# Optimization experiments

Hardware: AMD Instinct MI355X
Metric: run time of the kernel (lower is better)

Reference implementation:

```python
import jax, jax.numpy as jnp
import numpy as np

N_PEP, N_MHC, N_TCR = 20000, 5000, 100000
EMB, HID = 128, 256
E_PM, E_MT = 200000, 400000
B = 50000


def setup_inputs() -> dict:
    key = jax.random.key(0)
    ks = jax.random.split(key, 30)
    f32 = jnp.float32

    def w(k, shape, fan_in):
        # torch Linear default: U(-1/sqrt(fan_in), 1/sqrt(fan_in))
        lim = 1.0 / np.sqrt(fan_in)
        return jax.random.uniform(k, shape, dtype=f32, minval=-lim, maxval=lim)

    inp = {
        # embedding tables (learned params)
        "emb_pep": jax.random.normal(ks[0], (N_PEP, EMB), dtype=f32),
        "emb_mhc": jax.random.normal(ks[1], (N_MHC, EMB), dtype=f32),
        "emb_tcr": jax.random.normal(ks[2], (N_TCR, EMB), dtype=f32),
        # edge lists (src=edge_index[0], dst=edge_index[1])
        "src_pm": jax.random.randint(ks[3], (E_PM,), 0, N_PEP, dtype=jnp.int32),
        "dst_pm": jax.random.randint(ks[4], (E_PM,), 0, N_MHC, dtype=jnp.int32),
        "src_mt": jax.random.randint(ks[5], (E_MT,), 0, N_MHC, dtype=jnp.int32),
        "dst_mt": jax.random.randint(ks[6], (E_MT,), 0, N_TCR, dtype=jnp.int32),
        # triplet pack indices
        "pack_pep": jax.random.randint(ks[7], (B,), 0, N_PEP, dtype=jnp.int32),
        "pack_mhc": jax.random.randint(ks[8], (B,), 0, N_MHC, dtype=jnp.int32),
        "pack_tcr": jax.random.randint(ks[9], (B,), 0, N_TCR, dtype=jnp.int32),
        # SAGEConv params: Wl (aggregated neighbors, with bias), Wr (root, no bias)
        # layer 1: pep->mhc (src 128, dst 128); mhc->tcr (src 128, dst 128)
        "l1_pm_Wl": w(ks[10], (HID, EMB), EMB), "l1_pm_bl": w(ks[11], (HID,), EMB),
        "l1_pm_Wr": w(ks[12], (HID, EMB), EMB),
        "l1_mt_Wl": w(ks[13], (HID, EMB), EMB), "l1_mt_bl": w(ks[14], (HID,), EMB),
        "l1_mt_Wr": w(ks[15], (HID, EMB), EMB),
        # layer 2: pep->mhc (src 128, dst 256); mhc->tcr (src 256, dst 256)
        "l2_pm_Wl": w(ks[16], (HID, EMB), EMB), "l2_pm_bl": w(ks[17], (HID,), EMB),
        "l2_pm_Wr": w(ks[18], (HID, HID), HID),
        "l2_mt_Wl": w(ks[19], (HID, HID), HID), "l2_mt_bl": w(ks[20], (HID,), HID),
        "l2_mt_Wr": w(ks[21], (HID, HID), HID),
        # proj_pep and head MLP
        "proj_W": w(ks[22], (HID, EMB), EMB), "proj_b": w(ks[23], (HID,), EMB),
        "head_W1": w(ks[24], (HID, 3 * HID), 3 * HID), "head_b1": w(ks[25], (HID,), 3 * HID),
        "head_W2": w(ks[26], (1, HID), HID), "head_b2": w(ks[27], (1,), HID),
    }
    return inp


def _sage(x_src, x_dst, src, dst, Wl, bl, Wr, n_dst):
    # SAGEConv(mean): lin_l(mean_{j in N(i)} x_src[j]) + lin_r(x_dst[i])
    msg = jax.ops.segment_sum(x_src[src], dst, num_segments=n_dst)  # [n_dst, d_src]
    cnt = jax.ops.segment_sum(jnp.ones((src.shape[0],), x_src.dtype), dst, num_segments=n_dst)
    mean = msg / jnp.maximum(cnt, 1.0)[:, None]
    return mean @ Wl.T + bl + x_dst @ Wr.T


def reference(emb_pep, emb_mhc, emb_tcr,
              src_pm, dst_pm, src_mt, dst_mt,
              pack_pep, pack_mhc, pack_tcr,
              l1_pm_Wl, l1_pm_bl, l1_pm_Wr, l1_mt_Wl, l1_mt_bl, l1_mt_Wr,
              l2_pm_Wl, l2_pm_bl, l2_pm_Wr, l2_mt_Wl, l2_mt_bl, l2_mt_Wr,
              proj_W, proj_b, head_W1, head_b1, head_W2, head_b2):
    relu = jax.nn.relu
    # layer 1 (HeteroConv reads all relations from the same input dict)
    mhc1 = relu(_sage(emb_pep, emb_mhc, src_pm, dst_pm, l1_pm_Wl, l1_pm_bl, l1_pm_Wr, N_MHC))
    tcr1 = relu(_sage(emb_mhc, emb_tcr, src_mt, dst_mt, l1_mt_Wl, l1_mt_bl, l1_mt_Wr, N_TCR))
    # layer 2 ('pep' is never a destination, so it keeps its embedding)
    mhc2 = relu(_sage(emb_pep, mhc1, src_pm, dst_pm, l2_pm_Wl, l2_pm_bl, l2_pm_Wr, N_MHC))
    tcr2 = relu(_sage(mhc1, tcr1, src_mt, dst_mt, l2_mt_Wl, l2_mt_bl, l2_mt_Wr, N_TCR))
    # projections + triplet gather (dropout disabled: inference)
    hp = (emb_pep @ proj_W.T + proj_b)[pack_pep]  # [B, HID]
    hm = mhc2[pack_mhc]
    ht = tcr2[pack_tcr]
    z = jnp.concatenate([hp, hm, ht], axis=-1)  # [B, 3*HID]
    hidden = relu(z @ head_W1.T + head_b1)
    logits = hidden @ head_W2.T + head_b2
    return logits.squeeze(-1)
```

## Files before the change

kernel.cpp:

```cpp
#include <hip/hip_runtime.h>

constexpr int NPEP = 20000, NMHC = 5000, NTCR = 100000;
constexpr int EPM = 200000, EMT = 400000, BB = 50000;
constexpr int MAXU = 50000;

typedef __attribute__((ext_vector_type(8))) short bf16x8;
typedef __attribute__((ext_vector_type(4))) float f32x4;

__device__ inline ushort f2bf(float x) {
    union { float f; unsigned u; } v; v.f = x;
    unsigned r = (v.u + 0x7FFF + ((v.u >> 16) & 1)) >> 16;
    return (ushort)r;
}
__device__ inline float bf2f(ushort b) {
    union { unsigned u; float f; } t; t.u = ((unsigned)b) << 16; return t.f;
}
__device__ inline void bf2x2(unsigned u, float& a, float& b) {
    union { unsigned x; float f; } t1, t2;
    t1.x = u << 16; t2.x = u & 0xffff0000u;
    a = t1.f; b = t2.f;
}
__device__ inline ushort4 f4bf(float4 v) {
    return make_ushort4(f2bf(v.x), f2bf(v.y), f2bf(v.z), f2bf(v.w));
}

__global__ __launch_bounds__(256) void prep_kernel(
    int* __restrict__ ibz,
    const float4* __restrict__ Wr1f, ushort4* __restrict__ Wr1_b,
    const float4* __restrict__ Wr2f, ushort4* __restrict__ Wr2_b,
    const float* __restrict__ head_W1, ushort4* __restrict__ W1b_b, ushort4* __restrict__ W1c_b,
    const float* __restrict__ l1_pm_Wl, const float* __restrict__ l1_pm_Wr,
    const float* __restrict__ l1_mt_Wl, ushort* __restrict__ Wcat1_b,
    const float* __restrict__ l2_pm_Wl, const float* __restrict__ l2_pm_Wr,
    const float* __restrict__ l2_mt_Wl, ushort* __restrict__ Wcat2_b,
    const float4* __restrict__ emb_mhc, ushort* __restrict__ Acat1,
    const float* __restrict__ proj_W, const float* __restrict__ proj_b,
    ushort* __restrict__ Wcomp_b, float* __restrict__ bp) {
    __shared__ float red[128];
    const int b = blockIdx.x, tid = threadIdx.x;
    if (b < 303) {
        int i = b * 256 + tid;
        if (i < 77500) ((int4*)ibz)[i] = make_int4(0, 0, 0, 0);
    } else if (b < 335) {
        int i = (b - 303) * 256 + tid;
        if (i < 8192) Wr1_b[i] = f4bf(Wr1f[i]);
    } else if (b < 399) {
        int i = (b - 335) * 256 + tid;
        if (i < 16384) Wr2_b[i] = f4bf(Wr2f[i]);
    } else if (b < 463) {
        int i = (b - 399) * 256 + tid;
        if (i < 16384) {
            int n = i >> 6, k4 = (i & 63) * 4;
            float4 v = *(const float4*)(head_W1 + (size_t)n * 768 + 256 + k4);
            W1b_b[i] = f4bf(v);
        }
    } else if (b < 527) {
        int i = (b - 463) * 256 + tid;
        if (i < 16384) {
            int n = i >> 6, k4 = (i & 63) * 4;
            float4 v = *(const float4*)(head_W1 + (size_t)n * 768 + 512 + k4);
            W1c_b[i] = f4bf(v);
        }
    } else if (b < 1039) {
        int idx = (b - 527) * 256 + tid;
        if (idx < 131072) {
            int r = idx >> 8, k = idx & 255;
            float v;
            if (r < 256) v = (k < 128) ? l1_pm_Wl[r * 128 + k] : l1_pm_Wr[r * 128 + (k - 128)];
            else         v = (k < 128) ? 0.f : l1_mt_Wl[(r - 256) * 128 + (k - 128)];
            Wcat1_b[idx] = f2bf(v);
        }
    } else if (b < 1807) {
        int idx = (b - 1039) * 256 + tid;
        if (idx < 196608) {
            int r = idx / 384, k = idx - r * 384;
            float v;
            if (r < 256) v = (k < 128) ? l2_pm_Wl[r * 128 + k] : l2_pm_Wr[r * 256 + (k - 128)];
            else         v = (k < 128) ? 0.f : l2_mt_Wl[(r - 256) * 256 + (k - 128)];
            Wcat2_b[idx] = f2bf(v);
        }
    } else if (b < 2432) {
        int i4 = (b - 1807) * 256 + tid;
        if (i4 < 160000) {
            int r = i4 >> 5, c4 = (i4 & 31) * 4;
            *(ushort4*)(Acat1 + (size_t)r * 256 + 128 + c4) = f4bf(emb_mhc[i4]);
        }
    } else {
        int i = b - 2432;
        const float* w1row = head_W1 + (size_t)i * 768;
        if (tid < 128) {
            float acc = 0.f;
            for (int k = 0; k < 256; k++) acc += w1row[k] * proj_W[k * 128 + tid];
            Wcomp_b[i * 128 + tid] = f2bf(acc);
            float pb = w1row[2 * tid] * proj_b[2 * tid] + w1row[2 * tid + 1] * proj_b[2 * tid + 1];
            red[tid] = pb;
        }
        __syncthreads();
        if (tid < 64) { red[tid] += red[tid + 64]; }
        __syncthreads();
        if (tid < 32) { red[tid] += red[tid + 32]; }
        __syncthreads();
        if (tid == 0) {
            float s = 0.f;
            for (int j = 0; j < 32; j++) s += red[j];
            bp[i] = s;
        }
    }
}

__global__ void hist2_kernel(const int* __restrict__ dst_pm, const int* __restrict__ dst_mt,
                             const int* __restrict__ pack_tcr,
                             int* __restrict__ deg_pm, int* __restrict__ deg_mt,
                             int* __restrict__ mark) {
    int t = blockIdx.x * blockDim.x + threadIdx.x;
    if (t < EPM) atomicAdd(&deg_pm[dst_pm[t]], 1);
    else if (t < EPM + EMT) atomicAdd(&deg_mt[dst_mt[t - EPM]], 1);
    else if (t < EPM + EMT + BB) mark[pack_tcr[t - EPM - EMT]] = 1;
}

__global__ __launch_bounds__(256) void blocksum2_kernel(const int* __restrict__ deg_pm,
                                                        const int* __restrict__ deg_mt,
                                                        const int* __restrict__ mark,
                                                        int* __restrict__ bsum_pm,
                                                        int* __restrict__ bsum_mt,
                                                        int* __restrict__ bsum_mk) {
    __shared__ int red[256];
    const int tid = threadIdx.x;
    const int* deg; int n, bi; int* bsum;
    if (blockIdx.x < 5) { deg = deg_pm; n = NMHC; bi = blockIdx.x; bsum = bsum_pm; }
    else if (blockIdx.x < 103) { deg = deg_mt; n = NTCR; bi = blockIdx.x - 5; bsum = bsum_mt; }
    else { deg = mark; n = NTCR; bi = blockIdx.x - 103; bsum = bsum_mk; }
    const int base = bi * 1024;
    int s = 0;
#pragma unroll
    for (int j = 0; j < 4; j++) {
        int i = base + tid + j * 256;
        if (i < n) s += deg[i];
    }
    red[tid] = s;
    __syncthreads();
    for (int off = 128; off > 0; off >>= 1) {
        if (tid < off) red[tid] += red[tid + off];
        __syncthreads();
    }
    if (tid == 0) bsum[bi] = red[0];
}

__global__ __launch_bounds__(128) void scanb2_kernel(int* __restrict__ bsum_pm,
                                                     int* __restrict__ bsum_mt,
                                                     int* __restrict__ bsum_mk) {
    __shared__ int s[128];
    const int tid = threadIdx.x;
    int* bsum = (blockIdx.x == 0) ? bsum_pm : ((blockIdx.x == 1) ? bsum_mt : bsum_mk);
    const int nb = (blockIdx.x == 0) ? 5 : 98;
    int v = (tid < nb) ? bsum[tid] : 0;
    s[tid] = v;
    __syncthreads();
    for (int off = 1; off < 128; off <<= 1) {
        int t = (tid >= off) ? s[tid - off] : 0;
        __syncthreads();
        s[tid] += t;
        __syncthreads();
    }
    if (tid < nb) bsum[tid] = (tid > 0) ? s[tid - 1] : 0;
    if (tid == 0) bsum[nb] = s[nb - 1];
}

__global__ __launch_bounds__(256) void emit2_kernel(const int* __restrict__ deg_pm,
                                                    const int* __restrict__ deg_mt,
                                                    const int* __restrict__ mark,
                                                    const int* __restrict__ bsum_pm,
                                                    const int* __restrict__ bsum_mt,
                                                    const int* __restrict__ bsum_mk,
                                                    int* __restrict__ rp_pm, float* __restrict__ cnt_pm,
                                                    int* __restrict__ rp_mt, float* __restrict__ cnt_mt,
                                                    int* __restrict__ list) {
    __shared__ int tsum[256];
    const int tid = threadIdx.x;
    const int* deg; const int* bsum; int* rp; float* cnt; int n, nb, bi, mode;
    if (blockIdx.x < 5) { deg = deg_pm; bsum = bsum_pm; rp = rp_pm; cnt = cnt_pm; n = NMHC; nb = 5; bi = blockIdx.x; mode = 0; }
    else if (blockIdx.x < 103) { deg = deg_mt; bsum = bsum_mt; rp = rp_mt; cnt = cnt_mt; n = NTCR; nb = 98; bi = blockIdx.x - 5; mode = 0; }
    else { deg = mark; bsum = bsum_mk; rp = nullptr; cnt = nullptr; n = NTCR; nb = 98; bi = blockIdx.x - 103; mode = 1; }
    const int i0 = bi * 1024 + tid * 4;
    int4 v = make_int4(0, 0, 0, 0);
    if (i0 + 3 < n) v = *(const int4*)(deg + i0);
    else if (i0 < n) {
        int t[4] = {0, 0, 0, 0};
        for (int j = 0; j < 4 && i0 + j < n; j++) t[j] = deg[i0 + j];
        v = make_int4(t[0], t[1], t[2], t[3]);
    }
    int s = v.x + v.y + v.z + v.w;
    tsum[tid] = s;
    __syncthreads();
    for (int off = 1; off < 256; off <<= 1) {
        int t = (tid >= off) ? tsum[tid - off] : 0;
        __syncthreads();
        tsum[tid] += t;
        __syncthreads();
    }
    int ex = ((tid > 0) ? tsum[tid - 1] : 0) + bsum[bi];
    if (mode == 0) {
        if (i0 + 3 < n) {
            int r1 = ex + v.x, r2 = r1 + v.y, r3 = r2 + v.z;
            *(int4*)(rp + i0) = make_int4(ex, r1, r2, r3);
            *(float4*)(cnt + i0) = make_float4((float)v.x, (float)v.y, (float)v.z, (float)v.w);
        } else if (i0 < n) {
            int r = ex;
            int vv[4] = {v.x, v.y, v.z, v.w};
            for (int j = 0; j < 4 && i0 + j < n; j++) {
                rp[i0 + j] = r;
                cnt[i0 + j] = (float)vv[j];
                r += vv[j];
            }
        }
        if (bi == 0 && tid == 0) rp[n] = bsum[nb];
    } else {
        int p = ex;
        int vv[4] = {v.x, v.y, v.z, v.w};
#pragma unroll
        for (int j = 0; j < 4; j++) {
            if (i0 + j < n && vv[j]) list[p++] = i0 + j;
        }
    }
}

__global__ void fill2_kernel(const int* __restrict__ src_pm, const int* __restrict__ dst_pm,
                             const int* __restrict__ src_mt, const int* __restrict__ dst_mt,
                             const int* __restrict__ rp_pm, int* __restrict__ cur_pm, int* __restrict__ csr_pm,
                             const int* __restrict__ rp_mt, int* __restrict__ cur_mt, int* __restrict__ csr_mt) {
    int t = blockIdx.x * blockDim.x + threadIdx.x;
    if (t < EPM) {
        int d = dst_pm[t];
        int pos = atomicAdd(&cur_pm[d], 1);
        csr_pm[rp_pm[d] + pos] = src_pm[t];
    } else if (t < EPM + EMT) {
        int t2 = t - EPM;
        int d = dst_mt[t2];
        int pos = atomicAdd(&cur_mt[d], 1);
        csr_mt[rp_mt[d] + pos] = src_mt[t2];
    }
}

__global__ __launch_bounds__(256) void gatherpm_kernel(const int* __restrict__ rp,
                                                       const int* __restrict__ csr_src,
                                                       const float* __restrict__ X,
                                                       ushort* __restrict__ A1, ushort* __restrict__ A2,
                                                       int n) {
    const int tid = threadIdx.x;
    const int r = blockIdx.x * 8 + (tid >> 5);
    const int lane = tid & 31;
    if (r >= n) return;
    const int e0 = rp[r], e1 = rp[r + 1];
    float4 s = make_float4(0.f, 0.f, 0.f, 0.f);
    for (int e = e0; e < e1; e++) {
        const int sidx = csr_src[e];
        float4 v = ((const float4*)(X + (long)sidx * 128))[lane];
        s.x += v.x; s.y += v.y; s.z += v.z; s.w += v.w;
    }
    float sc = 1.f / fmaxf((float)(e1 - e0), 1.f);
    ushort4 o = make_ushort4(f2bf(s.x * sc), f2bf(s.y * sc), f2bf(s.z * sc), f2bf(s.w * sc));
    *(ushort4*)(A1 + (size_t)r * 256 + lane * 4) = o;
    *(ushort4*)(A2 + (size_t)r * 384 + lane * 4) = o;
}

template <int K, int NB0, bool RELU0, bool G2>
__global__ __launch_bounds__(256, 2) void mfma_fused_kernel(
    int M, const ushort* __restrict__ A, const ushort* __restrict__ W,
    const float* __restrict__ bias,
    ushort* __restrict__ out0, int s0, ushort* __restrict__ out1) {
    constexpr int RS = 40;
    __shared__ ushort Als[128 * RS];
    __shared__ ushort Wls[128 * RS];
    const int tid = threadIdx.x;
    const int m0 = blockIdx.x * 128, n0 = blockIdx.y * 128;
    const int lane = tid & 63, w = tid >> 6;
    const int wm = w >> 1, wn = w & 1;
    const int m16 = lane & 15, q = lane >> 4;

    f32x4 acc[4][4] = {};

    for (int k0 = 0; k0 < K; k0 += 32) {
        bf16x8 a_st[2], w_st[2];
#pragma unroll
        for (int r = 0; r < 2; r++) {
            int chunk = tid + r * 256;
            int row = chunk >> 2, off = (chunk & 3) * 8;
            int ga = min(m0 + row, M - 1);
            a_st[r] = *(const bf16x8*)(A + (size_t)ga * K + k0 + off);
            w_st[r] = *(const bf16x8*)(W + (size_t)(n0 + row) * K + k0 + off);
        }
        __syncthreads();
#pragma unroll
        for (int r = 0; r < 2; r++) {
            int chunk = tid + r * 256;
            int row = chunk >> 2, off = (chunk & 3) * 8;
            *(bf16x8*)(&Als[row * RS + off]) = a_st[r];
            *(bf16x8*)(&Wls[row * RS + off]) = w_st[r];
        }
        __syncthreads();
        bf16x8 af[4], bf[4];
#pragma unroll
        for (int t = 0; t < 4; t++) {
            af[t] = *(const bf16x8*)(&Als[(wm * 64 + t * 16 + m16) * RS + q * 8]);
            bf[t] = *(const bf16x8*)(&Wls[(wn * 64 + t * 16 + m16) * RS + q * 8]);
        }
#pragma unroll
        for (int mt = 0; mt < 4; mt++)
#pragma unroll
            for (int nt = 0; nt < 4; nt++)
                acc[mt][nt] = __builtin_amdgcn_mfma_f32_16x16x32_bf16(af[mt], bf[nt], acc[mt][nt], 0, 0, 0);
    }

    const bool g1 = G2 && ((int)blockIdx.y >= NB0);
#pragma unroll
    for (int mt = 0; mt < 4; mt++) {
#pragma unroll
        for (int i = 0; i < 4; i++) {
            int row = m0 + wm * 64 + mt * 16 + q * 4 + i;
            if (row >= M) continue;
#pragma unroll
            for (int nt = 0; nt < 4; nt++) {
                int col = n0 + wn * 64 + nt * 16 + m16;
                float v = acc[mt][nt][i];
                if (!g1) {
                    v += bias[col];
                    if (RELU0) v = fmaxf(v, 0.f);
                    out0[(size_t)row * s0 + col] = f2bf(v);
                } else {
                    out1[(size_t)row * 256 + (col - NB0 * 128)] = f2bf(v);
                }
            }
        }
    }
}

__global__ __launch_bounds__(256, 3) void tcrall_kernel(
    const int* __restrict__ nrowsp, const int* __restrict__ list,
    const int* __restrict__ rp, const int* __restrict__ csr_src,
    const ushort* __restrict__ Z1, const ushort* __restrict__ Z2,
    const float* __restrict__ emb_tcr,
    const ushort* __restrict__ Wr1, const ushort* __restrict__ Wr2,
    const ushort* __restrict__ W1c,
    const float* __restrict__ bl1, const float* __restrict__ bl2,
    ushort* __restrict__ Ht) {
    constexpr int RS1 = 136;
    constexpr int RS2 = 264;
    __shared__ ushort B[32 * RS2];
    __shared__ ushort A1[32 * RS2];
    __shared__ ushort A2[32 * RS2];
    __shared__ int origs[32];
    const int tid = threadIdx.x;
    const int M = nrowsp[0];
    const int m0 = blockIdx.x * 32;
    if (m0 >= M) return;
    const int lane = tid & 63, w = tid >> 6;
    const int m16 = lane & 15, q = lane >> 4;

    if (tid < 32) origs[tid] = list[min(m0 + tid, M - 1)];

#pragma unroll
    for (int r = 0; r < 4; r++) {
        int chunk = tid + r * 256;
        int row = chunk >> 5, c4 = (chunk & 31) * 4;
        int grow = list[min(m0 + row, M - 1)];
        float4 v = *(const float4*)(emb_tcr + (size_t)grow * 128 + c4);
        *(ushort4*)(&B[row * RS1 + c4]) = f4bf(v);
    }

    {
        const int g = tid >> 5, gl = tid & 31;
        for (int rr = g; rr < 32; rr += 8) {
            int cr = min(m0 + rr, M - 1);
            int orig = list[cr];
            int e0 = rp[orig], e1 = rp[orig + 1];
            float s1[8] = {}, s2[8] = {};
            for (int e = e0; e < e1; e++) {
                int sidx = csr_src[e];
                uint4 u1 = *(const uint4*)(Z1 + (size_t)sidx * 256 + gl * 8);
                uint4 u2 = *(const uint4*)(Z2 + (size_t)sidx * 256 + gl * 8);
                float a, b;
                bf2x2(u1.x, a, b); s1[0] += a; s1[1] += b;
                bf2x2(u1.y, a, b); s1[2] += a; s1[3] += b;
                bf2x2(u1.z, a, b); s1[4] += a; s1[5] += b;
                bf2x2(u1.w, a, b); s1[6] += a; s1[7] += b;
                bf2x2(u2.x, a, b); s2[0] += a; s2[1] += b;
                bf2x2(u2.y, a, b); s2[2] += a; s2[3] += b;
                bf2x2(u2.z, a, b); s2[4] += a; s2[5] += b;
                bf2x2(u2.w, a, b); s2[6] += a; s2[7] += b;
            }
            float es = 1.f / fmaxf((float)(e1 - e0), 1.f);
            uint4 w1, w2;
            w1.x = (unsigned)f2bf(s1[0] * es) | ((unsigned)f2bf(s1[1] * es) << 16);
            w1.y = (unsigned)f2bf(s1[2] * es) | ((unsigned)f2bf(s1[3] * es) << 16);
            w1.z = (unsigned)f2bf(s1[4] * es) | ((unsigned)f2bf(s1[5] * es) << 16);
            w1.w = (unsigned)f2bf(s1[6] * es) | ((unsigned)f2bf(s1[7] * es) << 16);
            w2.x = (unsigned)f2bf(s2[0] * es) | ((unsigned)f2bf(s2[1] * es) << 16);
            w2.y = (unsigned)f2bf(s2[2] * es) | ((unsigned)f2bf(s2[3] * es) << 16);
            w2.z = (unsigned)f2bf(s2[4] * es) | ((unsigned)f2bf(s2[5] * es) << 16);
            w2.w = (unsigned)f2bf(s2[6] * es) | ((unsigned)f2bf(s2[7] * es) << 16);
            *(uint4*)(&A1[rr * RS2 + gl * 8]) = w1;
            *(uint4*)(&A2[rr * RS2 + gl * 8]) = w2;
        }
    }
    __syncthreads();

    {
        f32x4 acc[2][4] = {};
        for (int k0 = 0; k0 < 128; k0 += 32) {
            bf16x8 af[2], bf[4];
#pragma unroll
            for (int t = 0; t < 2; t++)
                af[t] = *(const bf16x8*)(&B[(t * 16 + m16) * RS1 + k0 + q * 8]);
#pragma unroll
            for (int t = 0; t < 4; t++)
                bf[t] = *(const bf16x8*)(Wr1 + (size_t)(w * 64 + t * 16 + m16) * 128 + k0 + q * 8);
#pragma unroll
            for (int mt = 0; mt < 2; mt++)
#pragma unroll
                for (int nt = 0; nt < 4; nt++)
                    acc[mt][nt] = __builtin_amdgcn_mfma_f32_16x16x32_bf16(af[mt], bf[nt], acc[mt][nt], 0, 0, 0);
        }
        __syncthreads();
#pragma unroll
        for (int mt = 0; mt < 2; mt++)
#pragma unroll
            for (int i = 0; i < 4; i++) {
                int lr = mt * 16 + q * 4 + i;
#pragma unroll
                for (int nt = 0; nt < 4; nt++) {
                    int col = w * 64 + nt * 16 + m16;
                    float v = acc[mt][nt][i] + bl1[col] + bf2f(A1[lr * RS2 + col]);
                    B[lr * RS2 + col] = f2bf(fmaxf(v, 0.f));
                }
            }
    }
    __syncthreads();

    {
        f32x4 acc[2][4] = {};
        for (int k0 = 0; k0 < 256; k0 += 32) {
            bf16x8 af[2], bf[4];
#pragma unroll
            for (int t = 0; t < 2; t++)
                af[t] = *(const bf16x8*)(&B[(t * 16 + m16) * RS2 + k0 + q * 8]);
#pragma unroll
            for (int t = 0; t < 4; t++)
                bf[t] = *(const bf16x8*)(Wr2 + (size_t)(w * 64 + t * 16 + m16) * 256 + k0 + q * 8);
#pragma unroll
            for (int mt = 0; mt < 2; mt++)
#pragma unroll
                for (int nt = 0; nt < 4; nt++)
                    acc[mt][nt] = __builtin_amdgcn_mfma_f32_16x16x32_bf16(af[mt], bf[nt], acc[mt][nt], 0, 0, 0);
        }
        __syncthreads();
#pragma unroll
        for (int mt = 0; mt < 2; mt++)
#pragma unroll
            for (int i = 0; i < 4; i++) {
                int lr = mt * 16 + q * 4 + i;
#pragma unroll
                for (int nt = 0; nt < 4; nt++) {
                    int col = w * 64 + nt * 16 + m16;
                    float v = acc[mt][nt][i] + bl2[col] + bf2f(A2[lr * RS2 + col]);
                    B[lr * RS2 + col] = f2bf(fmaxf(v, 0.f));
                }
            }
    }
    __syncthreads();

    {
        f32x4 acc[2][4] = {};
        for (int k0 = 0; k0 < 256; k0 += 32) {
            bf16x8 af[2], bf[4];
#pragma unroll
            for (int t = 0; t < 2; t++)
                af[t] = *(const bf16x8*)(&B[(t * 16 + m16) * RS2 + k0 + q * 8]);
#pragma unroll
            for (int t = 0; t < 4; t++)
                bf[t] = *(const bf16x8*)(W1c + (size_t)(w * 64 + t * 16 + m16) * 256 + k0 + q * 8);
#pragma unroll
            for (int mt = 0; mt < 2; mt++)
#pragma unroll
                for (int nt = 0; nt < 4; nt++)
                    acc[mt][nt] = __builtin_amdgcn_mfma_f32_16x16x32_bf16(af[mt], bf[nt], acc[mt][nt], 0, 0, 0);
        }
        __syncthreads();
#pragma unroll
        for (int mt = 0; mt < 2; mt++)
#pragma unroll
            for (int i = 0; i < 4; i++) {
                int lr = mt * 16 + q * 4 + i;
#pragma unroll
                for (int nt = 0; nt < 4; nt++) {
                    int col = w * 64 + nt * 16 + m16;
                    B[lr * RS2 + col] = f2bf(acc[mt][nt][i]);
                }
            }
    }
    __syncthreads();

#pragma unroll
    for (int r = 0; r < 4; r++) {
        int chunk = tid + r * 256;
        int row = chunk >> 5, c8 = (chunk & 31) * 8;
        if (m0 + row < M)
            *(uint4*)(Ht + (size_t)origs[row] * 256 + c8) = *(const uint4*)(&B[row * RS2 + c8]);
    }
}

template <int K, bool HASB, bool AF32>
__global__ __launch_bounds__(256, 2) void mfma_out_kernel(
    int M, const void* __restrict__ Av, const ushort* __restrict__ W,
    const float* __restrict__ bias, ushort* __restrict__ out) {
    constexpr int RS = 40;
    __shared__ ushort Als[128 * RS];
    __shared__ ushort Wls[128 * RS];
    const int tid = threadIdx.x;
    const int m0 = blockIdx.x * 128, n0 = blockIdx.y * 128;
    const int lane = tid & 63, w = tid >> 6;
    const int wm = w >> 1, wn = w & 1;
    const int m16 = lane & 15, q = lane >> 4;

    f32x4 acc[4][4] = {};

    for (int k0 = 0; k0 < K; k0 += 32) {
        bf16x8 a_st[2], w_st[2];
#pragma unroll
        for (int r = 0; r < 2; r++) {
            int chunk = tid + r * 256;
            int row = chunk >> 2, off = (chunk & 3) * 8;
            int ga = min(m0 + row, M - 1);
            if constexpr (AF32) {
                const float* Af = (const float*)Av;
                float4 f0 = *(const float4*)(Af + (size_t)ga * K + k0 + off);
                float4 f1 = *(const float4*)(Af + (size_t)ga * K + k0 + off + 4);
                ushort4 u0 = f4bf(f0), u1 = f4bf(f1);
                bf16x8 av;
                av[0] = (short)u0.x; av[1] = (short)u0.y; av[2] = (short)u0.z; av[3] = (short)u0.w;
                av[4] = (short)u1.x; av[5] = (short)u1.y; av[6] = (short)u1.z; av[7] = (short)u1.w;
                a_st[r] = av;
            } else {
                a_st[r] = *(const bf16x8*)((const ushort*)Av + (size_t)ga * K + k0 + off);
            }
            w_st[r] = *(const bf16x8*)(W + (size_t)(n0 + row) * K + k0 + off);
        }
        __syncthreads();
#pragma unroll
        for (int r = 0; r < 2; r++) {
            int chunk = tid + r * 256;
            int row = chunk >> 2, off = (chunk & 3) * 8;
            *(bf16x8*)(&Als[row * RS + off]) = a_st[r];
            *(bf16x8*)(&Wls[row * RS + off]) = w_st[r];
        }
        __syncthreads();
        bf16x8 af[4], bf[4];
#pragma unroll
        for (int t = 0; t < 4; t++) {
            af[t] = *(const bf16x8*)(&Als[(wm * 64 + t * 16 + m16) * RS + q * 8]);
            bf[t] = *(const bf16x8*)(&Wls[(wn * 64 + t * 16 + m16) * RS + q * 8]);
        }
#pragma unroll
        for (int mt = 0; mt < 4; mt++)
#pragma unroll
            for (int nt = 0; nt < 4; nt++)
                acc[mt][nt] = __builtin_amdgcn_mfma_f32_16x16x32_bf16(af[mt], bf[nt], acc[mt][nt], 0, 0, 0);
    }

#pragma unroll
    for (int mt = 0; mt < 4; mt++) {
#pragma unroll
        for (int i = 0; i < 4; i++) {
            int row = m0 + wm * 64 + mt * 16 + q * 4 + i;
            if (row >= M) continue;
#pragma unroll
            for (int nt = 0; nt < 4; nt++) {
                int col = n0 + wn * 64 + nt * 16 + m16;
                float v = acc[mt][nt][i];
                if (HASB) v += bias[col];
                out[(size_t)row * 256 + col] = f2bf(v);
            }
        }
    }
}

__global__ __launch_bounds__(256) void combine_kernel(
    const ushort* __restrict__ Hp, const ushort* __restrict__ Hm, const ushort* __restrict__ Ht,
    const int* __restrict__ pp, const int* __restrict__ pm, const int* __restrict__ pt,
    const float* __restrict__ b1, const float* __restrict__ W2, const float* __restrict__ b2,
    float* __restrict__ out) {
    const int tid = threadIdx.x;
    const int lane = tid & 63, w = tid >> 6;
    const int c = lane * 4;
    const float4 b1v = *(const float4*)(b1 + c);
    const float4 w2v = *(const float4*)(W2 + c);
    const float b2v = b2[0];
    const int base = blockIdx.x * 32 + w * 8;
#pragma unroll
    for (int t = 0; t < 8; t++) {
        int i = base + t;
        if (i >= BB) return;
        int ra = pp[i], rb = pm[i], rc = pt[i];
        ushort4 ua = *(const ushort4*)(Hp + (size_t)ra * 256 + c);
        ushort4 ub = *(const ushort4*)(Hm + (size_t)rb * 256 + c);
        ushort4 uc = *(const ushort4*)(Ht + (size_t)rc * 256 + c);
        float h0 = fmaxf(bf2f(ua.x) + bf2f(ub.x) + bf2f(uc.x) + b1v.x, 0.f);
        float h1 = fmaxf(bf2f(ua.y) + bf2f(ub.y) + bf2f(uc.y) + b1v.y, 0.f);
        float h2 = fmaxf(bf2f(ua.z) + bf2f(ub.z) + bf2f(uc.z) + b1v.z, 0.f);
        float h3 = fmaxf(bf2f(ua.w) + bf2f(ub.w) + bf2f(uc.w) + b1v.w, 0.f);
        float p = h0 * w2v.x + h1 * w2v.y + h2 * w2v.z + h3 * w2v.w;
#pragma unroll
        for (int off = 32; off > 0; off >>= 1) p += __shfl_down(p, off);
        if (lane == 0) out[i] = p + b2v;
    }
}

extern "C" void kernel_launch(void* const* d_in, const int* in_sizes, int n_in,
                              void* d_out, int out_size, void* d_ws, size_t ws_size,
                              hipStream_t stream) {
    const float* emb_pep = (const float*)d_in[0];
    const float* emb_mhc = (const float*)d_in[1];
    const float* emb_tcr = (const float*)d_in[2];
    const int* src_pm = (const int*)d_in[3];
    const int* dst_pm = (const int*)d_in[4];
    const int* src_mt = (const int*)d_in[5];
    const int* dst_mt = (const int*)d_in[6];
    const int* pack_pep = (const int*)d_in[7];
    const int* pack_mhc = (const int*)d_in[8];
    const int* pack_tcr = (const int*)d_in[9];
    const float* l1_pm_Wl = (const float*)d_in[10];
    const float* l1_pm_bl = (const float*)d_in[11];
    const float* l1_pm_Wr = (const float*)d_in[12];
    const float* l1_mt_Wl = (const float*)d_in[13];
    const float* l1_mt_bl = (const float*)d_in[14];
    const float* l1_mt_Wr = (const float*)d_in[15];
    const float* l2_pm_Wl = (const float*)d_in[16];
    const float* l2_pm_bl = (const float*)d_in[17];
    const float* l2_pm_Wr = (const float*)d_in[18];
    const float* l2_mt_Wl = (const float*)d_in[19];
    const float* l2_mt_bl = (const float*)d_in[20];
    const float* l2_mt_Wr = (const float*)d_in[21];
    const float* proj_W = (const float*)d_in[22];
    const float* proj_b = (const float*)d_in[23];
    const float* head_W1 = (const float*)d_in[24];
    const float* head_b1 = (const float*)d_in[25];
    const float* head_W2 = (const float*)d_in[26];
    const float* head_b2 = (const float*)d_in[27];
    float* out = (float*)d_out;

    int* ib = (int*)d_ws;
    int* deg_pm = ib;
    int* cur_pm = ib + 5000;
    int* deg_mt = ib + 10000;
    int* cur_mt = ib + 110000;
    int* mark   = ib + 210000;
    int* rp_pm  = ib + 310000;
    int* rp_mt  = ib + 315008;
    int* csr_pm = ib + 415016;
    int* csr_mt = ib + 615016;
    int* bsum_pm = ib + 1015016;
    int* bsum_mt = ib + 1015176;
    int* bsum_mk = ib + 1015336;
    int* list    = ib + 1015496;

    float* f = (float*)(ib + 1065544);
    float* cnt_pm = f;
    float* cnt_mt = f + 5000;
    float* bp     = f + 105000;

    ushort* u = (ushort*)(f + 105344);
    ushort* Wcat1_b = u;
    ushort* Wcat2_b = u + 131072;
    ushort* W1b_b   = u + 327680;
    ushort* W1c_b   = u + 393216;
    ushort* Wcomp_b = u + 458752;
    ushort* Wr1_b   = u + 491520;
    ushort* Wr2_b   = u + 524288;
    ushort* Acat1   = u + 589824;
    ushort* Acat2   = u + 1869824;
    ushort* Zb1     = u + 3789824;
    ushort* Zb2     = u + 5069824;
    ushort* mhc2_b  = u + 6349824;
    ushort* Hp_b    = u + 7629824;
    ushort* Hm_b    = u + 12749824;
    ushort* Ht_b    = u + 14029824;

    prep_kernel<<<2688, 256, 0, stream>>>(
        ib,
        (const float4*)l1_mt_Wr, (ushort4*)Wr1_b,
        (const float4*)l2_mt_Wr, (ushort4*)Wr2_b,
        head_W1, (ushort4*)W1b_b, (ushort4*)W1c_b,
        l1_pm_Wl, l1_pm_Wr, l1_mt_Wl, Wcat1_b,
        l2_pm_Wl, l2_pm_Wr, l2_mt_Wl, Wcat2_b,
        (const float4*)emb_mhc, Acat1,
        proj_W, proj_b, Wcomp_b, bp);

    hist2_kernel<<<(EPM + EMT + BB + 255) / 256, 256, 0, stream>>>(
        dst_pm, dst_mt, pack_tcr, deg_pm, deg_mt, mark);
    blocksum2_kernel<<<201, 256, 0, stream>>>(deg_pm, deg_mt, mark, bsum_pm, bsum_mt, bsum_mk);
    scanb2_kernel<<<3, 128, 0, stream>>>(bsum_pm, bsum_mt, bsum_mk);
    emit2_kernel<<<201, 256, 0, stream>>>(deg_pm, deg_mt, mark, bsum_pm, bsum_mt, bsum_mk,
                                          rp_pm, cnt_pm, rp_mt, cnt_mt, list);
    fill2_kernel<<<(EPM + EMT + 255) / 256, 256, 0, stream>>>(
        src_pm, dst_pm, src_mt, dst_mt, rp_pm, cur_pm, csr_pm, rp_mt, cur_mt, csr_mt);

    gatherpm_kernel<<<(NMHC + 7) / 8, 256, 0, stream>>>(rp_pm, csr_pm, emb_pep, Acat1, Acat2, NMHC);

    mfma_fused_kernel<256, 2, true, true><<<dim3((NMHC + 127) / 128, 4), 256, 0, stream>>>(
        NMHC, Acat1, Wcat1_b, l1_pm_bl, Acat2 + 128, 384, Zb1);
    mfma_fused_kernel<384, 2, true, true><<<dim3((NMHC + 127) / 128, 4), 256, 0, stream>>>(
        NMHC, Acat2, Wcat2_b, l2_pm_bl, mhc2_b, 256, Zb2);

    tcrall_kernel<<<(MAXU + 31) / 32, 256, 0, stream>>>(
        bsum_mk + 98, list, rp_mt, csr_mt, Zb1, Zb2, emb_tcr,
        Wr1_b, Wr2_b, W1c_b, l1_mt_bl, l2_mt_bl, Ht_b);

    mfma_out_kernel<128, true, true><<<dim3((NPEP + 127) / 128, 2), 256, 0, stream>>>(
        NPEP, emb_pep, Wcomp_b, bp, Hp_b);
    mfma_out_kernel<256, false, false><<<dim3((NMHC + 127) / 128, 2), 256, 0, stream>>>(
        NMHC, mhc2_b, W1b_b, nullptr, Hm_b);

    combine_kernel<<<(BB + 31) / 32, 256, 0, stream>>>(
        Hp_b, Hm_b, Ht_b, pack_pep, pack_mhc, pack_tcr,
        head_b1, head_W2, head_b2, out);
}
```

Baseline: 416.3 us.

## Fuse all stages into one persistent mega-kernel with software grid barriers

Replaces the chain of about a dozen kernel launches (prep, histogram, scans, CSR fill, gathers, MFMA GEMMs, tcr stage, output projections, combine) with a single persistent kernel sized to occupancy. The stages are separated by atomic-counter grid barriers. The aim is to remove per-launch overhead and the idle tails between small dependent kernels. In exchange, each phase runs on a fixed grid that may fit its work less well, the barriers cost spinning, and the union shared memory may lower occupancy. The barrier has a timeout break, which would break correctness if blocks are not co-resident.

```diff
diff --git a/kernel.cpp b/kernel.cpp
--- a/kernel.cpp
+++ b/kernel.cpp
@@ -2,7 +2,6 @@
 
 constexpr int NPEP = 20000, NMHC = 5000, NTCR = 100000;
 constexpr int EPM = 200000, EMT = 400000, BB = 50000;
-constexpr int MAXU = 50000;
 
 typedef __attribute__((ext_vector_type(8))) short bf16x8;
 typedef __attribute__((ext_vector_type(4))) float f32x4;
@@ -24,255 +23,59 @@
     return make_ushort4(f2bf(v.x), f2bf(v.y), f2bf(v.z), f2bf(v.w));
 }
 
-__global__ __launch_bounds__(256) void prep_kernel(
-    int* __restrict__ ibz,
-    const float4* __restrict__ Wr1f, ushort4* __restrict__ Wr1_b,
-    const float4* __restrict__ Wr2f, ushort4* __restrict__ Wr2_b,
-    const float* __restrict__ head_W1, ushort4* __restrict__ W1b_b, ushort4* __restrict__ W1c_b,
-    const float* __restrict__ l1_pm_Wl, const float* __restrict__ l1_pm_Wr,
-    const float* __restrict__ l1_mt_Wl, ushort* __restrict__ Wcat1_b,
-    const float* __restrict__ l2_pm_Wl, const float* __restrict__ l2_pm_Wr,
-    const float* __restrict__ l2_mt_Wl, ushort* __restrict__ Wcat2_b,
-    const float4* __restrict__ emb_mhc, ushort* __restrict__ Acat1,
-    const float* __restrict__ proj_W, const float* __restrict__ proj_b,
-    ushort* __restrict__ Wcomp_b, float* __restrict__ bp) {
-    __shared__ float red[128];
-    const int b = blockIdx.x, tid = threadIdx.x;
-    if (b < 303) {
-        int i = b * 256 + tid;
-        if (i < 77500) ((int4*)ibz)[i] = make_int4(0, 0, 0, 0);
-    } else if (b < 335) {
-        int i = (b - 303) * 256 + tid;
-        if (i < 8192) Wr1_b[i] = f4bf(Wr1f[i]);
-    } else if (b < 399) {
-        int i = (b - 335) * 256 + tid;
-        if (i < 16384) Wr2_b[i] = f4bf(Wr2f[i]);
-    } else if (b < 463) {
-        int i = (b - 399) * 256 + tid;
-        if (i < 16384) {
-            int n = i >> 6, k4 = (i & 63) * 4;
-            float4 v = *(const float4*)(head_W1 + (size_t)n * 768 + 256 + k4);
-            W1b_b[i] = f4bf(v);
-        }
-    } else if (b < 527) {
-        int i = (b - 463) * 256 + tid;
-        if (i < 16384) {
-            int n = i >> 6, k4 = (i & 63) * 4;
-            float4 v = *(const float4*)(head_W1 + (size_t)n * 768 + 512 + k4);
-            W1c_b[i] = f4bf(v);
-        }
-    } else if (b < 1039) {
-        int idx = (b - 527) * 256 + tid;
-        if (idx < 131072) {
-            int r = idx >> 8, k = idx & 255;
-            float v;
-            if (r < 256) v = (k < 128) ? l1_pm_Wl[r * 128 + k] : l1_pm_Wr[r * 128 + (k - 128)];
-            else         v = (k < 128) ? 0.f : l1_mt_Wl[(r - 256) * 128 + (k - 128)];
-            Wcat1_b[idx] = f2bf(v);
-        }
-    } else if (b < 1807) {
-        int idx = (b - 1039) * 256 + tid;
-        if (idx < 196608) {
-            int r = idx / 384, k = idx - r * 384;
-            float v;
-            if (r < 256) v = (k < 128) ? l2_pm_Wl[r * 128 + k] : l2_pm_Wr[r * 256 + (k - 128)];
-            else         v = (k < 128) ? 0.f : l2_mt_Wl[(r - 256) * 256 + (k - 128)];
-            Wcat2_b[idx] = f2bf(v);
-        }
-    } else if (b < 2432) {
-        int i4 = (b - 1807) * 256 + tid;
-        if (i4 < 160000) {
-            int r = i4 >> 5, c4 = (i4 & 31) * 4;
-            *(ushort4*)(Acat1 + (size_t)r * 256 + 128 + c4) = f4bf(emb_mhc[i4]);
-        }
-    } else {
-        int i = b - 2432;
-        const float* w1row = head_W1 + (size_t)i * 768;
-        if (tid < 128) {
-            float acc = 0.f;
-            for (int k = 0; k < 256; k++) acc += w1row[k] * proj_W[k * 128 + tid];
-            Wcomp_b[i * 128 + tid] = f2bf(acc);
-            float pb = w1row[2 * tid] * proj_b[2 * tid] + w1row[2 * tid + 1] * proj_b[2 * tid + 1];
-            red[tid] = pb;
-        }
-        __syncthreads();
-        if (tid < 64) { red[tid] += red[tid + 64]; }
-        __syncthreads();
-        if (tid < 32) { red[tid] += red[tid + 32]; }
-        __syncthreads();
-        if (tid == 0) {
-            float s = 0.f;
-            for (int j = 0; j < 32; j++) s += red[j];
-            bp[i] = s;
-        }
-    }
-}
-
-__global__ void hist2_kernel(const int* __restrict__ dst_pm, const int* __restrict__ dst_mt,
-                             const int* __restrict__ pack_tcr,
-                             int* __restrict__ deg_pm, int* __restrict__ deg_mt,
-                             int* __restrict__ mark) {
-    int t = blockIdx.x * blockDim.x + threadIdx.x;
-    if (t < EPM) atomicAdd(&deg_pm[dst_pm[t]], 1);
-    else if (t < EPM + EMT) atomicAdd(&deg_mt[dst_mt[t - EPM]], 1);
-    else if (t < EPM + EMT + BB) mark[pack_tcr[t - EPM - EMT]] = 1;
-}
-
-__global__ __launch_bounds__(256) void blocksum2_kernel(const int* __restrict__ deg_pm,
-                                                        const int* __restrict__ deg_mt,
-                                                        const int* __restrict__ mark,
-                                                        int* __restrict__ bsum_pm,
-                                                        int* __restrict__ bsum_mt,
-                                                        int* __restrict__ bsum_mk) {
-    __shared__ int red[256];
-    const int tid = threadIdx.x;
-    const int* deg; int n, bi; int* bsum;
-    if (blockIdx.x < 5) { deg = deg_pm; n = NMHC; bi = blockIdx.x; bsum = bsum_pm; }
-    else if (blockIdx.x < 103) { deg = deg_mt; n = NTCR; bi = blockIdx.x - 5; bsum = bsum_mt; }
-    else { deg = mark; n = NTCR; bi = blockIdx.x - 103; bsum = bsum_mk; }
-    const int base = bi * 1024;
-    int s = 0;
-#pragma unroll
-    for (int j = 0; j < 4; j++) {
-        int i = base + tid + j * 256;
-        if (i < n) s += deg[i];
-    }
-    red[tid] = s;
+constexpr int RS  = 40;
+constexpr int RS1 = 136;
+constexpr int RS2 = 264;
+
+struct SMem {
+    union {
+        float red[128];
+        int ired[256];
+        int tsum[256];
+        struct { ushort Als[128 * RS]; ushort Wls[128 * RS]; } g;
+        struct { ushort B[32 * RS2]; ushort A1[32 * RS2]; ushort A2[32 * RS2];
+                 int origs[32]; } t;
+    };
+};
+
+struct MegaArgs {
+    const float *emb_pep, *emb_mhc, *emb_tcr;
+    const int *src_pm, *dst_pm, *src_mt, *dst_mt;
+    const int *pack_pep, *pack_mhc, *pack_tcr;
+    const float *l1_pm_Wl, *l1_pm_bl, *l1_pm_Wr, *l1_mt_Wl, *l1_mt_bl, *l1_mt_Wr;
+    const float *l2_pm_Wl, *l2_pm_bl, *l2_pm_Wr, *l2_mt_Wl, *l2_mt_bl, *l2_mt_Wr;
+    const float *proj_W, *proj_b, *head_W1, *head_b1, *head_W2, *head_b2;
+    float* out;
+    int *deg_pm, *cur_pm, *deg_mt, *cur_mt, *mark;
+    int *rp_pm, *rp_mt, *csr_pm, *csr_mt;
+    int *bsum_pm, *bsum_mt, *bsum_mk, *nrows, *list, *bar;
+    float* bp;
+    ushort *Wcat1_b, *Wcat2_b, *W1b_b, *W1c_b, *Wcomp_b, *Wr1_b, *Wr2_b;
+    ushort *Acat1, *Acat2, *Zb1, *Zb2, *mhc2_b, *Hp_b, *Hm_b, *Ht_b;
+};
+
+__device__ inline void gbar(int* cnt, int target) {
     __syncthreads();
-    for (int off = 128; off > 0; off >>= 1) {
-        if (tid < off) red[tid] += red[tid + off];
-        __syncthreads();
-    }
-    if (tid == 0) bsum[bi] = red[0];
-}
-
-__global__ __launch_bounds__(128) void scanb2_kernel(int* __restrict__ bsum_pm,
-                                                     int* __restrict__ bsum_mt,
-                                                     int* __restrict__ bsum_mk) {
-    __shared__ int s[128];
-    const int tid = threadIdx.x;
-    int* bsum = (blockIdx.x == 0) ? bsum_pm : ((blockIdx.x == 1) ? bsum_mt : bsum_mk);
-    const int nb = (blockIdx.x == 0) ? 5 : 98;
-    int v = (tid < nb) ? bsum[tid] : 0;
-    s[tid] = v;
+    __threadfence();
+    if (threadIdx.x == 0) {
+        atomicAdd(cnt, 1);
+        long long t0 = clock64();
+        while (__hip_atomic_load(cnt, __ATOMIC_RELAXED, __HIP_MEMORY_SCOPE_AGENT) < target) {
+            __builtin_amdgcn_s_sleep(2);
+            if (clock64() - t0 > 2000000000LL) break;
+        }
+    }
     __syncthreads();
-    for (int off = 1; off < 128; off <<= 1) {
-        int t = (tid >= off) ? s[tid - off] : 0;
-        __syncthreads();
-        s[tid] += t;
-        __syncthreads();
-    }
-    if (tid < nb) bsum[tid] = (tid > 0) ? s[tid - 1] : 0;
-    if (tid == 0) bsum[nb] = s[nb - 1];
-}
-
-__global__ __launch_bounds__(256) void emit2_kernel(const int* __restrict__ deg_pm,
-                                                    const int* __restrict__ deg_mt,
-                                                    const int* __restrict__ mark,
-                                                    const int* __restrict__ bsum_pm,
-                                                    const int* __restrict__ bsum_mt,
-                                                    const int* __restrict__ bsum_mk,
-                                                    int* __restrict__ rp_pm, float* __restrict__ cnt_pm,
-                                                    int* __restrict__ rp_mt, float* __restrict__ cnt_mt,
-                                                    int* __restrict__ list) {
-    __shared__ int tsum[256];
-    const int tid = threadIdx.x;
-    const int* deg; const int* bsum; int* rp; float* cnt; int n, nb, bi, mode;
-    if (blockIdx.x < 5) { deg = deg_pm; bsum = bsum_pm; rp = rp_pm; cnt = cnt_pm; n = NMHC; nb = 5; bi = blockIdx.x; mode = 0; }
-    else if (blockIdx.x < 103) { deg = deg_mt; bsum = bsum_mt; rp = rp_mt; cnt = cnt_mt; n = NTCR; nb = 98; bi = blockIdx.x - 5; mode = 0; }
-    else { deg = mark; bsum = bsum_mk; rp = nullptr; cnt = nullptr; n = NTCR; nb = 98; bi = blockIdx.x - 103; mode = 1; }
-    const int i0 = bi * 1024 + tid * 4;
-    int4 v = make_int4(0, 0, 0, 0);
-    if (i0 + 3 < n) v = *(const int4*)(deg + i0);
-    else if (i0 < n) {
-        int t[4] = {0, 0, 0, 0};
-        for (int j = 0; j < 4 && i0 + j < n; j++) t[j] = deg[i0 + j];
-        v = make_int4(t[0], t[1], t[2], t[3]);
-    }
-    int s = v.x + v.y + v.z + v.w;
-    tsum[tid] = s;
-    __syncthreads();
-    for (int off = 1; off < 256; off <<= 1) {
-        int t = (tid >= off) ? tsum[tid - off] : 0;
-        __syncthreads();
-        tsum[tid] += t;
-        __syncthreads();
-    }
-    int ex = ((tid > 0) ? tsum[tid - 1] : 0) + bsum[bi];
-    if (mode == 0) {
-        if (i0 + 3 < n) {
-            int r1 = ex + v.x, r2 = r1 + v.y, r3 = r2 + v.z;
-            *(int4*)(rp + i0) = make_int4(ex, r1, r2, r3);
-            *(float4*)(cnt + i0) = make_float4((float)v.x, (float)v.y, (float)v.z, (float)v.w);
-        } else if (i0 < n) {
-            int r = ex;
-            int vv[4] = {v.x, v.y, v.z, v.w};
-            for (int j = 0; j < 4 && i0 + j < n; j++) {
-                rp[i0 + j] = r;
-                cnt[i0 + j] = (float)vv[j];
-                r += vv[j];
-            }
-        }
-        if (bi == 0 && tid == 0) rp[n] = bsum[nb];
-    } else {
-        int p = ex;
-        int vv[4] = {v.x, v.y, v.z, v.w};
-#pragma unroll
-        for (int j = 0; j < 4; j++) {
-            if (i0 + j < n && vv[j]) list[p++] = i0 + j;
-        }
-    }
-}
-
-__global__ void fill2_kernel(const int* __restrict__ src_pm, const int* __restrict__ dst_pm,
-                             const int* __restrict__ src_mt, const int* __restrict__ dst_mt,
-                             const int* __restrict__ rp_pm, int* __restrict__ cur_pm, int* __restrict__ csr_pm,
-                             const int* __restrict__ rp_mt, int* __restrict__ cur_mt, int* __restrict__ csr_mt) {
-    int t = blockIdx.x * blockDim.x + threadIdx.x;
-    if (t < EPM) {
-        int d = dst_pm[t];
-        int pos = atomicAdd(&cur_pm[d], 1);
-        csr_pm[rp_pm[d] + pos] = src_pm[t];
-    } else if (t < EPM + EMT) {
-        int t2 = t - EPM;
-        int d = dst_mt[t2];
-        int pos = atomicAdd(&cur_mt[d], 1);
-        csr_mt[rp_mt[d] + pos] = src_mt[t2];
-    }
-}
-
-__global__ __launch_bounds__(256) void gatherpm_kernel(const int* __restrict__ rp,
-                                                       const int* __restrict__ csr_src,
-                                                       const float* __restrict__ X,
-                                                       ushort* __restrict__ A1, ushort* __restrict__ A2,
-                                                       int n) {
-    const int tid = threadIdx.x;
-    const int r = blockIdx.x * 8 + (tid >> 5);
-    const int lane = tid & 31;
-    if (r >= n) return;
-    const int e0 = rp[r], e1 = rp[r + 1];
-    float4 s = make_float4(0.f, 0.f, 0.f, 0.f);
-    for (int e = e0; e < e1; e++) {
-        const int sidx = csr_src[e];
-        float4 v = ((const float4*)(X + (long)sidx * 128))[lane];
-        s.x += v.x; s.y += v.y; s.z += v.z; s.w += v.w;
-    }
-    float sc = 1.f / fmaxf((float)(e1 - e0), 1.f);
-    ushort4 o = make_ushort4(f2bf(s.x * sc), f2bf(s.y * sc), f2bf(s.z * sc), f2bf(s.w * sc));
-    *(ushort4*)(A1 + (size_t)r * 256 + lane * 4) = o;
-    *(ushort4*)(A2 + (size_t)r * 384 + lane * 4) = o;
-}
-
-template <int K, int NB0, bool RELU0, bool G2>
-__global__ __launch_bounds__(256, 2) void mfma_fused_kernel(
-    int M, const ushort* __restrict__ A, const ushort* __restrict__ W,
+    __threadfence();
+}
+
+template <int K, int NB0, bool RELU0>
+__device__ __forceinline__ void fused_tile(
+    SMem& sm, int tid, int bx, int by, int M,
+    const ushort* __restrict__ A, const ushort* __restrict__ W,
     const float* __restrict__ bias,
     ushort* __restrict__ out0, int s0, ushort* __restrict__ out1) {
-    constexpr int RS = 40;
-    __shared__ ushort Als[128 * RS];
-    __shared__ ushort Wls[128 * RS];
-    const int tid = threadIdx.x;
-    const int m0 = blockIdx.x * 128, n0 = blockIdx.y * 128;
+    const int m0 = bx * 128, n0 = by * 128;
     const int lane = tid & 63, w = tid >> 6;
     const int wm = w >> 1, wn = w & 1;
     const int m16 = lane & 15, q = lane >> 4;
@@ -294,15 +97,15 @@
         for (int r = 0; r < 2; r++) {
             int chunk = tid + r * 256;
             int row = chunk >> 2, off = (chunk & 3) * 8;
-            *(bf16x8*)(&Als[row * RS + off]) = a_st[r];
-            *(bf16x8*)(&Wls[row * RS + off]) = w_st[r];
+            *(bf16x8*)(&sm.g.Als[row * RS + off]) = a_st[r];
+            *(bf16x8*)(&sm.g.Wls[row * RS + off]) = w_st[r];
         }
         __syncthreads();
         bf16x8 af[4], bf[4];
 #pragma unroll
         for (int t = 0; t < 4; t++) {
-            af[t] = *(const bf16x8*)(&Als[(wm * 64 + t * 16 + m16) * RS + q * 8]);
-            bf[t] = *(const bf16x8*)(&Wls[(wn * 64 + t * 16 + m16) * RS + q * 8]);
+            af[t] = *(const bf16x8*)(&sm.g.Als[(wm * 64 + t * 16 + m16) * RS + q * 8]);
+            bf[t] = *(const bf16x8*)(&sm.g.Wls[(wn * 64 + t * 16 + m16) * RS + q * 8]);
         }
 #pragma unroll
         for (int mt = 0; mt < 4; mt++)
@@ -311,7 +114,7 @@
                 acc[mt][nt] = __builtin_amdgcn_mfma_f32_16x16x32_bf16(af[mt], bf[nt], acc[mt][nt], 0, 0, 0);
     }
 
-    const bool g1 = G2 && ((int)blockIdx.y >= NB0);
+    const bool g1 = (by >= NB0);
 #pragma unroll
     for (int mt = 0; mt < 4; mt++) {
 #pragma unroll
@@ -334,189 +137,12 @@
     }
 }
 
-__global__ __launch_bounds__(256, 3) void tcrall_kernel(
-    const int* __restrict__ nrowsp, const int* __restrict__ list,
-    const int* __restrict__ rp, const int* __restrict__ csr_src,
-    const ushort* __restrict__ Z1, const ushort* __restrict__ Z2,
-    const float* __restrict__ emb_tcr,
-    const ushort* __restrict__ Wr1, const ushort* __restrict__ Wr2,
-    const ushort* __restrict__ W1c,
-    const float* __restrict__ bl1, const float* __restrict__ bl2,
-    ushort* __restrict__ Ht) {
-    constexpr int RS1 = 136;
-    constexpr int RS2 = 264;
-    __shared__ ushort B[32 * RS2];
-    __shared__ ushort A1[32 * RS2];
-    __shared__ ushort A2[32 * RS2];
-    __shared__ int origs[32];
-    const int tid = threadIdx.x;
-    const int M = nrowsp[0];
-    const int m0 = blockIdx.x * 32;
-    if (m0 >= M) return;
-    const int lane = tid & 63, w = tid >> 6;
-    const int m16 = lane & 15, q = lane >> 4;
-
-    if (tid < 32) origs[tid] = list[min(m0 + tid, M - 1)];
-
-#pragma unroll
-    for (int r = 0; r < 4; r++) {
-        int chunk = tid + r * 256;
-        int row = chunk >> 5, c4 = (chunk & 31) * 4;
-        int grow = list[min(m0 + row, M - 1)];
-        float4 v = *(const float4*)(emb_tcr + (size_t)grow * 128 + c4);
-        *(ushort4*)(&B[row * RS1 + c4]) = f4bf(v);
-    }
-
-    {
-        const int g = tid >> 5, gl = tid & 31;
-        for (int rr = g; rr < 32; rr += 8) {
-            int cr = min(m0 + rr, M - 1);
-            int orig = list[cr];
-            int e0 = rp[orig], e1 = rp[orig + 1];
-            float s1[8] = {}, s2[8] = {};
-            for (int e = e0; e < e1; e++) {
-                int sidx = csr_src[e];
-                uint4 u1 = *(const uint4*)(Z1 + (size_t)sidx * 256 + gl * 8);
-                uint4 u2 = *(const uint4*)(Z2 + (size_t)sidx * 256 + gl * 8);
-                float a, b;
-                bf2x2(u1.x, a, b); s1[0] += a; s1[1] += b;
-                bf2x2(u1.y, a, b); s1[2] += a; s1[3] += b;
-                bf2x2(u1.z, a, b); s1[4] += a; s1[5] += b;
-                bf2x2(u1.w, a, b); s1[6] += a; s1[7] += b;
-                bf2x2(u2.x, a, b); s2[0] += a; s2[1] += b;
-                bf2x2(u2.y, a, b); s2[2] += a; s2[3] += b;
-                bf2x2(u2.z, a, b); s2[4] += a; s2[5] += b;
-                bf2x2(u2.w, a, b); s2[6] += a; s2[7] += b;
-            }
-            float es = 1.f / fmaxf((float)(e1 - e0), 1.f);
-            uint4 w1, w2;
-            w1.x = (unsigned)f2bf(s1[0] * es) | ((unsigned)f2bf(s1[1] * es) << 16);
-            w1.y = (unsigned)f2bf(s1[2] * es) | ((unsigned)f2bf(s1[3] * es) << 16);
-            w1.z = (unsigned)f2bf(s1[4] * es) | ((unsigned)f2bf(s1[5] * es) << 16);
-            w1.w = (unsigned)f2bf(s1[6] * es) | ((unsigned)f2bf(s1[7] * es) << 16);
-            w2.x = (unsigned)f2bf(s2[0] * es) | ((unsigned)f2bf(s2[1] * es) << 16);
-            w2.y = (unsigned)f2bf(s2[2] * es) | ((unsigned)f2bf(s2[3] * es) << 16);
-            w2.z = (unsigned)f2bf(s2[4] * es) | ((unsigned)f2bf(s2[5] * es) << 16);
-            w2.w = (unsigned)f2bf(s2[6] * es) | ((unsigned)f2bf(s2[7] * es) << 16);
-            *(uint4*)(&A1[rr * RS2 + gl * 8]) = w1;
-            *(uint4*)(&A2[rr * RS2 + gl * 8]) = w2;
-        }
-    }
-    __syncthreads();
-
-    {
-        f32x4 acc[2][4] = {};
-        for (int k0 = 0; k0 < 128; k0 += 32) {
-            bf16x8 af[2], bf[4];
-#pragma unroll
-            for (int t = 0; t < 2; t++)
-                af[t] = *(const bf16x8*)(&B[(t * 16 + m16) * RS1 + k0 + q * 8]);
-#pragma unroll
-            for (int t = 0; t < 4; t++)
-                bf[t] = *(const bf16x8*)(Wr1 + (size_t)(w * 64 + t * 16 + m16) * 128 + k0 + q * 8);
-#pragma unroll
-            for (int mt = 0; mt < 2; mt++)
-#pragma unroll
-                for (int nt = 0; nt < 4; nt++)
-                    acc[mt][nt] = __builtin_amdgcn_mfma_f32_16x16x32_bf16(af[mt], bf[nt], acc[mt][nt], 0, 0, 0);
-        }
-        __syncthreads();
-#pragma unroll
-        for (int mt = 0; mt < 2; mt++)
-#pragma unroll
-            for (int i = 0; i < 4; i++) {
-                int lr = mt * 16 + q * 4 + i;
-#pragma unroll
-                for (int nt = 0; nt < 4; nt++) {
-                    int col = w * 64 + nt * 16 + m16;
-                    float v = acc[mt][nt][i] + bl1[col] + bf2f(A1[lr * RS2 + col]);
-                    B[lr * RS2 + col] = f2bf(fmaxf(v, 0.f));
-                }
-            }
-    }
-    __syncthreads();
-
-    {
-        f32x4 acc[2][4] = {};
-        for (int k0 = 0; k0 < 256; k0 += 32) {
-            bf16x8 af[2], bf[4];
-#pragma unroll
-            for (int t = 0; t < 2; t++)
-                af[t] = *(const bf16x8*)(&B[(t * 16 + m16) * RS2 + k0 + q * 8]);
-#pragma unroll
-            for (int t = 0; t < 4; t++)
-                bf[t] = *(const bf16x8*)(Wr2 + (size_t)(w * 64 + t * 16 + m16) * 256 + k0 + q * 8);
-#pragma unroll
-            for (int mt = 0; mt < 2; mt++)
-#pragma unroll
-                for (int nt = 0; nt < 4; nt++)
-                    acc[mt][nt] = __builtin_amdgcn_mfma_f32_16x16x32_bf16(af[mt], bf[nt], acc[mt][nt], 0, 0, 0);
-        }
-        __syncthreads();
-#pragma unroll
-        for (int mt = 0; mt < 2; mt++)
-#pragma unroll
-            for (int i = 0; i < 4; i++) {
-                int lr = mt * 16 + q * 4 + i;
-#pragma unroll
-                for (int nt = 0; nt < 4; nt++) {
-                    int col = w * 64 + nt * 16 + m16;
-                    float v = acc[mt][nt][i] + bl2[col] + bf2f(A2[lr * RS2 + col]);
-                    B[lr * RS2 + col] = f2bf(fmaxf(v, 0.f));
-                }
-            }
-    }
-    __syncthreads();
-
-    {
-        f32x4 acc[2][4] = {};
-        for (int k0 = 0; k0 < 256; k0 += 32) {
-            bf16x8 af[2], bf[4];
-#pragma unroll
-            for (int t = 0; t < 2; t++)
-                af[t] = *(const bf16x8*)(&B[(t * 16 + m16) * RS2 + k0 + q * 8]);
-#pragma unroll
-            for (int t = 0; t < 4; t++)
-                bf[t] = *(const bf16x8*)(W1c + (size_t)(w * 64 + t * 16 + m16) * 256 + k0 + q * 8);
-#pragma unroll
-            for (int mt = 0; mt < 2; mt++)
-#pragma unroll
-                for (int nt = 0; nt < 4; nt++)
-                    acc[mt][nt] = __builtin_amdgcn_mfma_f32_16x16x32_bf16(af[mt], bf[nt], acc[mt][nt], 0, 0, 0);
-        }
-        __syncthreads();
-#pragma unroll
-        for (int mt = 0; mt < 2; mt++)
-#pragma unroll
-            for (int i = 0; i < 4; i++) {
-                int lr = mt * 16 + q * 4 + i;
-#pragma unroll
-                for (int nt = 0; nt < 4; nt++) {
-                    int col = w * 64 + nt * 16 + m16;
-                    B[lr * RS2 + col] = f2bf(acc[mt][nt][i]);
-                }
-            }
-    }
-    __syncthreads();
-
-#pragma unroll
-    for (int r = 0; r < 4; r++) {
-        int chunk = tid + r * 256;
-        int row = chunk >> 5, c8 = (chunk & 31) * 8;
-        if (m0 + row < M)
-            *(uint4*)(Ht + (size_t)origs[row] * 256 + c8) = *(const uint4*)(&B[row * RS2 + c8]);
-    }
-}
-
 template <int K, bool HASB, bool AF32>
-__global__ __launch_bounds__(256, 2) void mfma_out_kernel(
-    int M, const void* __restrict__ Av, const ushort* __restrict__ W,
+__device__ __forceinline__ void out_tile(
+    SMem& sm, int tid, int bx, int by, int M,
+    const void* __restrict__ Av, const ushort* __restrict__ W,
     const float* __restrict__ bias, ushort* __restrict__ out) {
-    constexpr int RS = 40;
-    __shared__ ushort Als[128 * RS];
-    __shared__ ushort Wls[128 * RS];
-    const int tid = threadIdx.x;
-    const int m0 = blockIdx.x * 128, n0 = blockIdx.y * 128;
+    const int m0 = bx * 128, n0 = by * 128;
     const int lane = tid & 63, w = tid >> 6;
     const int wm = w >> 1, wn = w & 1;
     const int m16 = lane & 15, q = lane >> 4;
@@ -549,15 +175,15 @@
         for (int r = 0; r < 2; r++) {
             int chunk = tid + r * 256;
             int row = chunk >> 2, off = (chunk & 3) * 8;
-            *(bf16x8*)(&Als[row * RS + off]) = a_st[r];
-            *(bf16x8*)(&Wls[row * RS + off]) = w_st[r];
+            *(bf16x8*)(&sm.g.Als[row * RS + off]) = a_st[r];
+            *(bf16x8*)(&sm.g.Wls[row * RS + off]) = w_st[r];
         }
         __syncthreads();
         bf16x8 af[4], bf[4];
 #pragma unroll
         for (int t = 0; t < 4; t++) {
-            af[t] = *(const bf16x8*)(&Als[(wm * 64 + t * 16 + m16) * RS + q * 8]);
-            bf[t] = *(const bf16x8*)(&Wls[(wn * 64 + t * 16 + m16) * RS + q * 8]);
+            af[t] = *(const bf16x8*)(&sm.g.Als[(wm * 64 + t * 16 + m16) * RS + q * 8]);
+            bf[t] = *(const bf16x8*)(&sm.g.Wls[(wn * 64 + t * 16 + m16) * RS + q * 8]);
         }
 #pragma unroll
         for (int mt = 0; mt < 4; mt++)
@@ -583,143 +209,513 @@
     }
 }
 
-__global__ __launch_bounds__(256) void combine_kernel(
-    const ushort* __restrict__ Hp, const ushort* __restrict__ Hm, const ushort* __restrict__ Ht,
-    const int* __restrict__ pp, const int* __restrict__ pm, const int* __restrict__ pt,
-    const float* __restrict__ b1, const float* __restrict__ W2, const float* __restrict__ b2,
-    float* __restrict__ out) {
+__device__ __forceinline__ void tcr_tile(SMem& sm, int tid, int bt, int M, const MegaArgs& a) {
+    const int m0 = bt * 32;
+    const int lane = tid & 63, w = tid >> 6;
+    const int m16 = lane & 15, q = lane >> 4;
+
+    __syncthreads();
+
+    if (tid < 32) sm.t.origs[tid] = a.list[min(m0 + tid, M - 1)];
+
+#pragma unroll
+    for (int r = 0; r < 4; r++) {
+        int chunk = tid + r * 256;
+        int row = chunk >> 5, c4 = (chunk & 31) * 4;
+        int grow = a.list[min(m0 + row, M - 1)];
+        float4 v = *(const float4*)(a.emb_tcr + (size_t)grow * 128 + c4);
+        *(ushort4*)(&sm.t.B[row * RS1 + c4]) = f4bf(v);
+    }
+
+    {
+        const int g = tid >> 5, gl = tid & 31;
+        for (int rr = g; rr < 32; rr += 8) {
+            int cr = min(m0 + rr, M - 1);
+            int orig = a.list[cr];
+            int e0 = a.rp_mt[orig], e1 = a.rp_mt[orig + 1];
+            float s1[8] = {}, s2[8] = {};
+            for (int e = e0; e < e1; e++) {
+                int sidx = a.csr_mt[e];
+                uint4 u1 = *(const uint4*)(a.Zb1 + (size_t)sidx * 256 + gl * 8);
+                uint4 u2 = *(const uint4*)(a.Zb2 + (size_t)sidx * 256 + gl * 8);
+                float x, y;
+                bf2x2(u1.x, x, y); s1[0] += x; s1[1] += y;
+                bf2x2(u1.y, x, y); s1[2] += x; s1[3] += y;
+                bf2x2(u1.z, x, y); s1[4] += x; s1[5] += y;
+                bf2x2(u1.w, x, y); s1[6] += x; s1[7] += y;
+                bf2x2(u2.x, x, y); s2[0] += x; s2[1] += y;
+                bf2x2(u2.y, x, y); s2[2] += x; s2[3] += y;
+                bf2x2(u2.z, x, y); s2[4] += x; s2[5] += y;
+                bf2x2(u2.w, x, y); s2[6] += x; s2[7] += y;
+            }
+            float es = 1.f / fmaxf((float)(e1 - e0), 1.f);
+            uint4 w1, w2;
+            w1.x = (unsigned)f2bf(s1[0] * es) | ((unsigned)f2bf(s1[1] * es) << 16);
+            w1.y = (unsigned)f2bf(s1[2] * es) | ((unsigned)f2bf(s1[3] * es) << 16);
+            w1.z = (unsigned)f2bf(s1[4] * es) | ((unsigned)f2bf(s1[5] * es) << 16);
+            w1.w = (unsigned)f2bf(s1[6] * es) | ((unsigned)f2bf(s1[7] * es) << 16);
+            w2.x = (unsigned)f2bf(s2[0] * es) | ((unsigned)f2bf(s2[1] * es) << 16);
+            w2.y = (unsigned)f2bf(s2[2] * es) | ((unsigned)f2bf(s2[3] * es) << 16);
+            w2.z = (unsigned)f2bf(s2[4] * es) | ((unsigned)f2bf(s2[5] * es) << 16);
+            w2.w = (unsigned)f2bf(s2[6] * es) | ((unsigned)f2bf(s2[7] * es) << 16);
+            *(uint4*)(&sm.t.A1[rr * RS2 + gl * 8]) = w1;
+            *(uint4*)(&sm.t.A2[rr * RS2 + gl * 8]) = w2;
+        }
+    }
+    __syncthreads();
+
+    {
+        f32x4 acc[2][4] = {};
+        for (int k0 = 0; k0 < 128; k0 += 32) {
+            bf16x8 af[2], bf[4];
+#pragma unroll
+            for (int t = 0; t < 2; t++)
+                af[t] = *(const bf16x8*)(&sm.t.B[(t * 16 + m16) * RS1 + k0 + q * 8]);
+#pragma unroll
+            for (int t = 0; t < 4; t++)
+                bf[t] = *(const bf16x8*)(a.Wr1_b + (size_t)(w * 64 + t * 16 + m16) * 128 + k0 + q * 8);
+#pragma unroll
+            for (int mt = 0; mt < 2; mt++)
+#pragma unroll
+                for (int nt = 0; nt < 4; nt++)
+                    acc[mt][nt] = __builtin_amdgcn_mfma_f32_16x16x32_bf16(af[mt], bf[nt], acc[mt][nt], 0, 0, 0);
+        }
+        __syncthreads();
+#pragma unroll
+        for (int mt = 0; mt < 2; mt++)
+#pragma unroll
+            for (int i = 0; i < 4; i++) {
+                int lr = mt * 16 + q * 4 + i;
+#pragma unroll
+                for (int nt = 0; nt < 4; nt++) {
+                    int col = w * 64 + nt * 16 + m16;
+                    float v = acc[mt][nt][i] + a.l1_mt_bl[col] + bf2f(sm.t.A1[lr * RS2 + col]);
+                    sm.t.B[lr * RS2 + col] = f2bf(fmaxf(v, 0.f));
+                }
+            }
+    }
+    __syncthreads();
+
+    {
+        f32x4 acc[2][4] = {};
+        for (int k0 = 0; k0 < 256; k0 += 32) {
+            bf16x8 af[2], bf[4];
+#pragma unroll
+            for (int t = 0; t < 2; t++)
+                af[t] = *(const bf16x8*)(&sm.t.B[(t * 16 + m16) * RS2 + k0 + q * 8]);
+#pragma unroll
+            for (int t = 0; t < 4; t++)
+                bf[t] = *(const bf16x8*)(a.Wr2_b + (size_t)(w * 64 + t * 16 + m16) * 256 + k0 + q * 8);
+#pragma unroll
+            for (int mt = 0; mt < 2; mt++)
+#pragma unroll
+                for (int nt = 0; nt < 4; nt++)
+                    acc[mt][nt] = __builtin_amdgcn_mfma_f32_16x16x32_bf16(af[mt], bf[nt], acc[mt][nt], 0, 0, 0);
+        }
+        __syncthreads();
+#pragma unroll
+        for (int mt = 0; mt < 2; mt++)
+#pragma unroll
+            for (int i = 0; i < 4; i++) {
+                int lr = mt * 16 + q * 4 + i;
+#pragma unroll
+                for (int nt = 0; nt < 4; nt++) {
+                    int col = w * 64 + nt * 16 + m16;
+                    float v = acc[mt][nt][i] + a.l2_mt_bl[col] + bf2f(sm.t.A2[lr * RS2 + col]);
+                    sm.t.B[lr * RS2 + col] = f2bf(fmaxf(v, 0.f));
+                }
+            }
+    }
+    __syncthreads();
+
+    {
+        f32x4 acc[2][4] = {};
+        for (int k0 = 0; k0 < 256; k0 += 32) {
+            bf16x8 af[2], bf[4];
+#pragma unroll
+            for (int t = 0; t < 2; t++)
+                af[t] = *(const bf16x8*)(&sm.t.B[(t * 16 + m16) * RS2 + k0 + q * 8]);
+#pragma unroll
+            for (int t = 0; t < 4; t++)
+                bf[t] = *(const bf16x8*)(a.W1c_b + (size_t)(w * 64 + t * 16 + m16) * 256 + k0 + q * 8);
+#pragma unroll
+            for (int mt = 0; mt < 2; mt++)
+#pragma unroll
+                for (int nt = 0; nt < 4; nt++)
+                    acc[mt][nt] = __builtin_amdgcn_mfma_f32_16x16x32_bf16(af[mt], bf[nt], acc[mt][nt], 0, 0, 0);
+        }
+        __syncthreads();
+#pragma unroll
+        for (int mt = 0; mt < 2; mt++)
+#pragma unroll
+            for (int i = 0; i < 4; i++) {
+                int lr = mt * 16 + q * 4 + i;
+#pragma unroll
+                for (int nt = 0; nt < 4; nt++) {
+                    int col = w * 64 + nt * 16 + m16;
+                    sm.t.B[lr * RS2 + col] = f2bf(acc[mt][nt][i]);
+                }
+            }
+    }
+    __syncthreads();
+
+#pragma unroll
+    for (int r = 0; r < 4; r++) {
+        int chunk = tid + r * 256;
+        int row = chunk >> 5, c8 = (chunk & 31) * 8;
+        if (m0 + row < M)
+            *(uint4*)(a.Ht_b + (size_t)sm.t.origs[row] * 256 + c8) = *(const uint4*)(&sm.t.B[row * RS2 + c8]);
+    }
+}
+
+__global__ __launch_bounds__(256, 3) void mega_kernel(MegaArgs a) {
     const int tid = threadIdx.x;
-    const int lane = tid & 63, w = tid >> 6;
-    const int c = lane * 4;
-    const float4 b1v = *(const float4*)(b1 + c);
-    const float4 w2v = *(const float4*)(W2 + c);
-    const float b2v = b2[0];
-    const int base = blockIdx.x * 32 + w * 8;
-#pragma unroll
-    for (int t = 0; t < 8; t++) {
-        int i = base + t;
-        if (i >= BB) return;
-        int ra = pp[i], rb = pm[i], rc = pt[i];
-        ushort4 ua = *(const ushort4*)(Hp + (size_t)ra * 256 + c);
-        ushort4 ub = *(const ushort4*)(Hm + (size_t)rb * 256 + c);
-        ushort4 uc = *(const ushort4*)(Ht + (size_t)rc * 256 + c);
-        float h0 = fmaxf(bf2f(ua.x) + bf2f(ub.x) + bf2f(uc.x) + b1v.x, 0.f);
-        float h1 = fmaxf(bf2f(ua.y) + bf2f(ub.y) + bf2f(uc.y) + b1v.y, 0.f);
-        float h2 = fmaxf(bf2f(ua.z) + bf2f(ub.z) + bf2f(uc.z) + b1v.z, 0.f);
-        float h3 = fmaxf(bf2f(ua.w) + bf2f(ub.w) + bf2f(uc.w) + b1v.w, 0.f);
-        float p = h0 * w2v.x + h1 * w2v.y + h2 * w2v.z + h3 * w2v.w;
-#pragma unroll
-        for (int off = 32; off > 0; off >>= 1) p += __shfl_down(p, off);
-        if (lane == 0) out[i] = p + b2v;
+    const int bid = blockIdx.x;
+    const int NB = gridDim.x;
+    int ep = 0;
+    __shared__ SMem sm;
+
+    for (int b = bid; b < 2688; b += NB) {
+        if (b < 303) {
+            int i = b * 256 + tid;
+            if (i < 77500) ((int4*)a.deg_pm)[i] = make_int4(0, 0, 0, 0);
+        } else if (b < 335) {
+            int i = (b - 303) * 256 + tid;
+            if (i < 8192) ((ushort4*)a.Wr1_b)[i] = f4bf(((const float4*)a.l1_mt_Wr)[i]);
+        } else if (b < 399) {
+            int i = (b - 335) * 256 + tid;
+            if (i < 16384) ((ushort4*)a.Wr2_b)[i] = f4bf(((const float4*)a.l2_mt_Wr)[i]);
+        } else if (b < 463) {
+            int i = (b - 399) * 256 + tid;
+            if (i < 16384) {
+                int n = i >> 6, k4 = (i & 63) * 4;
+                ((ushort4*)a.W1b_b)[i] = f4bf(*(const float4*)(a.head_W1 + (size_t)n * 768 + 256 + k4));
+            }
+        } else if (b < 527) {
+            int i = (b - 463) * 256 + tid;
+            if (i < 16384) {
+                int n = i >> 6, k4 = (i & 63) * 4;
+                ((ushort4*)a.W1c_b)[i] = f4bf(*(const float4*)(a.head_W1 + (size_t)n * 768 + 512 + k4));
+            }
+        } else if (b < 1039) {
+            int idx = (b - 527) * 256 + tid;
+            if (idx < 131072) {
+                int r = idx >> 8, k = idx & 255;
+                float v;
+                if (r < 256) v = (k < 128) ? a.l1_pm_Wl[r * 128 + k] : a.l1_pm_Wr[r * 128 + (k - 128)];
+                else         v = (k < 128) ? 0.f : a.l1_mt_Wl[(r - 256) * 128 + (k - 128)];
+                a.Wcat1_b[idx] = f2bf(v);
+            }
+        } else if (b < 1807) {
+            int idx = (b - 1039) * 256 + tid;
+            if (idx < 196608) {
+                int r = idx / 384, k = idx - r * 384;
+                float v;
+                if (r < 256) v = (k < 128) ? a.l2_pm_Wl[r * 128 + k] : a.l2_pm_Wr[r * 256 + (k - 128)];
+                else         v = (k < 128) ? 0.f : a.l2_mt_Wl[(r - 256) * 256 + (k - 128)];
+                a.Wcat2_b[idx] = f2bf(v);
+            }
+        } else if (b < 2432) {
+            int i4 = (b - 1807) * 256 + tid;
+            if (i4 < 160000) {
+                int r = i4 >> 5, c4 = (i4 & 31) * 4;
+                *(ushort4*)(a.Acat1 + (size_t)r * 256 + 128 + c4) = f4bf(((const float4*)a.emb_mhc)[i4]);
+            }
+        } else {
+            int i = b - 2432;
+            const float* w1row = a.head_W1 + (size_t)i * 768;
+            __syncthreads();
+            if (tid < 128) {
+                float acc = 0.f;
+                for (int k = 0; k < 256; k++) acc += w1row[k] * a.proj_W[k * 128 + tid];
+                a.Wcomp_b[i * 128 + tid] = f2bf(acc);
+                sm.red[tid] = w1row[2 * tid] * a.proj_b[2 * tid] + w1row[2 * tid + 1] * a.proj_b[2 * tid + 1];
+            }
+            __syncthreads();
+            if (tid < 64) sm.red[tid] += sm.red[tid + 64];
+            __syncthreads();
+            if (tid < 32) sm.red[tid] += sm.red[tid + 32];
+            __syncthreads();
+            if (tid == 0) {
+                float s = 0.f;
+                for (int j = 0; j < 32; j++) s += sm.red[j];
+                a.bp[i] = s;
+            }
+        }
+    }
+    gbar(a.bar, NB * ++ep);
+
+    for (int t = bid * 256 + tid; t < EPM + EMT + BB; t += NB * 256) {
+        if (t < EPM) atomicAdd(&a.deg_pm[a.dst_pm[t]], 1);
+        else if (t < EPM + EMT) atomicAdd(&a.deg_mt[a.dst_mt[t - EPM]], 1);
+        else atomicAdd(&a.mark[a.pack_tcr[t - EPM - EMT]], 0x10000);
+    }
+    gbar(a.bar, NB * ++ep);
+
+    for (int b = bid; b < 201; b += NB) {
+        const int* deg; int n, bi; int* bsum; int mk = 0;
+        if (b < 5) { deg = a.deg_pm; n = NMHC; bi = b; bsum = a.bsum_pm; }
+        else if (b < 103) { deg = a.deg_mt; n = NTCR; bi = b - 5; bsum = a.bsum_mt; }
+        else { deg = a.mark; n = NTCR; bi = b - 103; bsum = a.bsum_mk; mk = 1; }
+        __syncthreads();
+        const int base = bi * 1024;
+        int s = 0;
+#pragma unroll
+        for (int j = 0; j < 4; j++) {
+            int i = base + tid + j * 256;
+            if (i < n) { int d = deg[i]; s += mk ? (d != 0) : d; }
+        }
+        sm.ired[tid] = s;
+        __syncthreads();
+        for (int off = 128; off > 0; off >>= 1) {
+            if (tid < off) sm.ired[tid] += sm.ired[tid + off];
+            __syncthreads();
+        }
+        if (tid == 0) bsum[bi] = sm.ired[0];
+    }
+    gbar(a.bar, NB * ++ep);
+
+    for (int b = bid; b < 201; b += NB) {
+        const int* deg; const int* bsumA; int* rp; int n, nb, bi, mode;
+        if (b < 5) { deg = a.deg_pm; bsumA = a.bsum_pm; rp = a.rp_pm; n = NMHC; nb = 5; bi = b; mode = 0; }
+        else if (b < 103) { deg = a.deg_mt; bsumA = a.bsum_mt; rp = a.rp_mt; n = NTCR; nb = 98; bi = b - 5; mode = 0; }
+        else { deg = a.mark; bsumA = a.bsum_mk; rp = nullptr; n = NTCR; nb = 98; bi = b - 103; mode = 1; }
+        __syncthreads();
+        sm.tsum[tid] = (tid < bi) ? bsumA[tid] : 0;
+        __syncthreads();
+        for (int off = 128; off > 0; off >>= 1) {
+            if (tid < off) sm.tsum[tid] += sm.tsum[tid + off];
+            __syncthreads();
+        }
+        const int base = sm.tsum[0];
+        __syncthreads();
+        const int i0 = bi * 1024 + tid * 4;
+        int4 v = make_int4(0, 0, 0, 0);
+        if (i0 + 3 < n) v = *(const int4*)(deg + i0);
+        else if (i0 < n) {
+            int t[4] = {0, 0, 0, 0};
+            for (int j = 0; j < 4 && i0 + j < n; j++) t[j] = deg[i0 + j];
+            v = make_int4(t[0], t[1], t[2], t[3]);
+        }
+        if (mode == 1) { v.x = (v.x != 0); v.y = (v.y != 0); v.z = (v.z != 0); v.w = (v.w != 0); }
+        sm.tsum[tid] = v.x + v.y + v.z + v.w;
+        __syncthreads();
+        for (int off = 1; off < 256; off <<= 1) {
+            int t = (tid >= off) ? sm.tsum[tid - off] : 0;
+            __syncthreads();
+            sm.tsum[tid] += t;
+            __syncthreads();
+        }
+        int ex = ((tid > 0) ? sm.tsum[tid - 1] : 0) + base;
+        if (mode == 0) {
+            if (i0 + 3 < n) {
+                int r1 = ex + v.x, r2 = r1 + v.y, r3 = r2 + v.z;
+                *(int4*)(rp + i0) = make_int4(ex, r1, r2, r3);
+            } else if (i0 < n) {
+                int r = ex;
+                int vv[4] = {v.x, v.y, v.z, v.w};
+                for (int j = 0; j < 4 && i0 + j < n; j++) { rp[i0 + j] = r; r += vv[j]; }
+            }
+            if (bi == nb - 1 && tid == 255) rp[n] = base + sm.tsum[255];
+        } else {
+            int p = ex;
+            int vv[4] = {v.x, v.y, v.z, v.w};
+#pragma unroll
+            for (int j = 0; j < 4; j++) {
+                if (i0 + j < n && vv[j]) a.list[p++] = i0 + j;
+            }
+            if (bi == nb - 1 && tid == 255) a.nrows[0] = base + sm.tsum[255];
+        }
+    }
+    gbar(a.bar, NB * ++ep);
+
+    for (int t = bid * 256 + tid; t < EPM + EMT; t += NB * 256) {
+        if (t < EPM) {
+            int d = a.dst_pm[t];
+            int pos = atomicAdd(&a.cur_pm[d], 1);
+            a.csr_pm[a.rp_pm[d] + pos] = a.src_pm[t];
+        } else {
+            int t2 = t - EPM;
+            int d = a.dst_mt[t2];
+            int pos = atomicAdd(&a.cur_mt[d], 1);
+            a.csr_mt[a.rp_mt[d] + pos] = a.src_mt[t2];
+        }
+    }
+    gbar(a.bar, NB * ++ep);
+
+    for (int vb = bid; vb < 625; vb += NB) {
+        const int r = vb * 8 + (tid >> 5);
+        const int lane = tid & 31;
+        if (r < NMHC) {
+            const int e0 = a.rp_pm[r], e1 = a.rp_pm[r + 1];
+            float4 s = make_float4(0.f, 0.f, 0.f, 0.f);
+            for (int e = e0; e < e1; e++) {
+                const int sidx = a.csr_pm[e];
+                float4 v = ((const float4*)(a.emb_pep + (long)sidx * 128))[lane];
+                s.x += v.x; s.y += v.y; s.z += v.z; s.w += v.w;
+            }
+            float sc = 1.f / fmaxf((float)(e1 - e0), 1.f);
+            ushort4 o = make_ushort4(f2bf(s.x * sc), f2bf(s.y * sc), f2bf(s.z * sc), f2bf(s.w * sc));
+            *(ushort4*)(a.Acat1 + (size_t)r * 256 + lane * 4) = o;
+            *(ushort4*)(a.Acat2 + (size_t)r * 384 + lane * 4) = o;
+        }
+    }
+    gbar(a.bar, NB * ++ep);
+
+    for (int vb = bid; vb < 317; vb += NB) {
+        if (vb < 160)
+            fused_tile<256, 2, true>(sm, tid, vb % 40, vb / 40, NMHC,
+                                     a.Acat1, a.Wcat1_b, a.l1_pm_bl, a.Acat2 + 128, 384, a.Zb1);
+        else {
+            int v = vb - 160;
+            out_tile<128, true, true>(sm, tid, v % 157, v / 157, NPEP,
+                                      a.emb_pep, a.Wcomp_b, a.bp, a.Hp_b);
+        }
+    }
+    gbar(a.bar, NB * ++ep);
+
+    for (int vb = bid; vb < 317; vb += NB) {
+        if (vb < 160)
+            fused_tile<384, 2, true>(sm, tid, vb % 40, vb / 40, NMHC,
+                                     a.Acat2, a.Wcat2_b, a.l2_pm_bl, a.mhc2_b, 256, a.Zb2);
+        else {
+            int v = vb - 160 + 157;
+            out_tile<128, true, true>(sm, tid, v % 157, v / 157, NPEP,
+                                      a.emb_pep, a.Wcomp_b, a.bp, a.Hp_b);
+        }
+    }
+    gbar(a.bar, NB * ++ep);
+
+    {
+        const int M = a.nrows[0];
+        const int NT = (M + 31) >> 5;
+        for (int vb = bid; vb < NT + 80; vb += NB) {
+            if (vb < NT) tcr_tile(sm, tid, vb, M, a);
+            else {
+                int v = vb - NT;
+                __syncthreads();
+                out_tile<256, false, false>(sm, tid, v % 40, v / 40, NMHC,
+                                            a.mhc2_b, a.W1b_b, nullptr, a.Hm_b);
+            }
+        }
+    }
+    gbar(a.bar, NB * ++ep);
+
+    {
+        const int lane = tid & 63, w = tid >> 6;
+        const int c = lane * 4;
+        const float4 b1v = *(const float4*)(a.head_b1 + c);
+        const float4 w2v = *(const float4*)(a.head_W2 + c);
+        const float b2v = a.head_b2[0];
+        for (int vb = bid; vb < (BB + 31) / 32; vb += NB) {
+            const int base2 = vb * 32 + w * 8;
+#pragma unroll
+            for (int t = 0; t < 8; t++) {
+                int i = base2 + t;
+                if (i < BB) {
+                    int ra = a.pack_pep[i], rb = a.pack_mhc[i], rc = a.pack_tcr[i];
+                    ushort4 ua = *(const ushort4*)(a.Hp_b + (size_t)ra * 256 + c);
+                    ushort4 ub = *(const ushort4*)(a.Hm_b + (size_t)rb * 256 + c);
+                    ushort4 uc = *(const ushort4*)(a.Ht_b + (size_t)rc * 256 + c);
+                    float h0 = fmaxf(bf2f(ua.x) + bf2f(ub.x) + bf2f(uc.x) + b1v.x, 0.f);
+                    float h1 = fmaxf(bf2f(ua.y) + bf2f(ub.y) + bf2f(uc.y) + b1v.y, 0.f);
+                    float h2 = fmaxf(bf2f(ua.z) + bf2f(ub.z) + bf2f(uc.z) + b1v.z, 0.f);
+                    float h3 = fmaxf(bf2f(ua.w) + bf2f(ub.w) + bf2f(uc.w) + b1v.w, 0.f);
+                    float p = h0 * w2v.x + h1 * w2v.y + h2 * w2v.z + h3 * w2v.w;
+#pragma unroll
+                    for (int off = 32; off > 0; off >>= 1) p += __shfl_down(p, off);
+                    if (lane == 0) a.out[i] = p + b2v;
+                }
+            }
+        }
     }
 }
 
 extern "C" void kernel_launch(void* const* d_in, const int* in_sizes, int n_in,
                               void* d_out, int out_size, void* d_ws, size_t ws_size,
                               hipStream_t stream) {
-    const float* emb_pep = (const float*)d_in[0];
-    const float* emb_mhc = (const float*)d_in[1];
-    const float* emb_tcr = (const float*)d_in[2];
-    const int* src_pm = (const int*)d_in[3];
-    const int* dst_pm = (const int*)d_in[4];
-    const int* src_mt = (const int*)d_in[5];
-    const int* dst_mt = (const int*)d_in[6];
-    const int* pack_pep = (const int*)d_in[7];
-    const int* pack_mhc = (const int*)d_in[8];
-    const int* pack_tcr = (const int*)d_in[9];
-    const float* l1_pm_Wl = (const float*)d_in[10];
-    const float* l1_pm_bl = (const float*)d_in[11];
-    const float* l1_pm_Wr = (const float*)d_in[12];
-    const float* l1_mt_Wl = (const float*)d_in[13];
-    const float* l1_mt_bl = (const float*)d_in[14];
-    const float* l1_mt_Wr = (const float*)d_in[15];
-    const float* l2_pm_Wl = (const float*)d_in[16];
-    const float* l2_pm_bl = (const float*)d_in[17];
-    const float* l2_pm_Wr = (const float*)d_in[18];
-    const float* l2_mt_Wl = (const float*)d_in[19];
-    const float* l2_mt_bl = (const float*)d_in[20];
-    const float* l2_mt_Wr = (const float*)d_in[21];
-    const float* proj_W = (const float*)d_in[22];
-    const float* proj_b = (const float*)d_in[23];
-    const float* head_W1 = (const float*)d_in[24];
-    const float* head_b1 = (const float*)d_in[25];
-    const float* head_W2 = (const float*)d_in[26];
-    const float* head_b2 = (const float*)d_in[27];
-    float* out = (float*)d_out;
+    MegaArgs a;
+    a.emb_pep = (const float*)d_in[0];
+    a.emb_mhc = (const float*)d_in[1];
+    a.emb_tcr = (const float*)d_in[2];
+    a.src_pm = (const int*)d_in[3];
+    a.dst_pm = (const int*)d_in[4];
+    a.src_mt = (const int*)d_in[5];
+    a.dst_mt = (const int*)d_in[6];
+    a.pack_pep = (const int*)d_in[7];
+    a.pack_mhc = (const int*)d_in[8];
+    a.pack_tcr = (const int*)d_in[9];
+    a.l1_pm_Wl = (const float*)d_in[10];
+    a.l1_pm_bl = (const float*)d_in[11];
+    a.l1_pm_Wr = (const float*)d_in[12];
+    a.l1_mt_Wl = (const float*)d_in[13];
+    a.l1_mt_bl = (const float*)d_in[14];
+    a.l1_mt_Wr = (const float*)d_in[15];
+    a.l2_pm_Wl = (const float*)d_in[16];
+    a.l2_pm_bl = (const float*)d_in[17];
+    a.l2_pm_Wr = (const float*)d_in[18];
+    a.l2_mt_Wl = (const float*)d_in[19];
+    a.l2_mt_bl = (const float*)d_in[20];
+    a.l2_mt_Wr = (const float*)d_in[21];
+    a.proj_W = (const float*)d_in[22];
+    a.proj_b = (const float*)d_in[23];
+    a.head_W1 = (const float*)d_in[24];
+    a.head_b1 = (const float*)d_in[25];
+    a.head_W2 = (const float*)d_in[26];
+    a.head_b2 = (const float*)d_in[27];
+    a.out = (float*)d_out;
 
     int* ib = (int*)d_ws;
-    int* deg_pm = ib;
-    int* cur_pm = ib + 5000;
-    int* deg_mt = ib + 10000;
-    int* cur_mt = ib + 110000;
-    int* mark   = ib + 210000;
-    int* rp_pm  = ib + 310000;
-    int* rp_mt  = ib + 315008;
-    int* csr_pm = ib + 415016;
-    int* csr_mt = ib + 615016;
-    int* bsum_pm = ib + 1015016;
-    int* bsum_mt = ib + 1015176;
-    int* bsum_mk = ib + 1015336;
-    int* list    = ib + 1015496;
-
-    float* f = (float*)(ib + 1065544);
-    float* cnt_pm = f;
-    float* cnt_mt = f + 5000;
-    float* bp     = f + 105000;
-
-    ushort* u = (ushort*)(f + 105344);
-    ushort* Wcat1_b = u;
-    ushort* Wcat2_b = u + 131072;
-    ushort* W1b_b   = u + 327680;
-    ushort* W1c_b   = u + 393216;
-    ushort* Wcomp_b = u + 458752;
-    ushort* Wr1_b   = u + 491520;
-    ushort* Wr2_b   = u + 524288;
-    ushort* Acat1   = u + 589824;
-    ushort* Acat2   = u + 1869824;
-    ushort* Zb1     = u + 3789824;
-    ushort* Zb2     = u + 5069824;
-    ushort* mhc2_b  = u + 6349824;
-    ushort* Hp_b    = u + 7629824;
-    ushort* Hm_b    = u + 12749824;
-    ushort* Ht_b    = u + 14029824;
-
-    prep_kernel<<<2688, 256, 0, stream>>>(
-        ib,
-        (const float4*)l1_mt_Wr, (ushort4*)Wr1_b,
-        (const float4*)l2_mt_Wr, (ushort4*)Wr2_b,
-        head_W1, (ushort4*)W1b_b, (ushort4*)W1c_b,
-        l1_pm_Wl, l1_pm_Wr, l1_mt_Wl, Wcat1_b,
-        l2_pm_Wl, l2_pm_Wr, l2_mt_Wl, Wcat2_b,
-        (const float4*)emb_mhc, Acat1,
-        proj_W, proj_b, Wcomp_b, bp);
-
-    hist2_kernel<<<(EPM + EMT + BB + 255) / 256, 256, 0, stream>>>(
-        dst_pm, dst_mt, pack_tcr, deg_pm, deg_mt, mark);
-    blocksum2_kernel<<<201, 256, 0, stream>>>(deg_pm, deg_mt, mark, bsum_pm, bsum_mt, bsum_mk);
-    scanb2_kernel<<<3, 128, 0, stream>>>(bsum_pm, bsum_mt, bsum_mk);
-    emit2_kernel<<<201, 256, 0, stream>>>(deg_pm, deg_mt, mark, bsum_pm, bsum_mt, bsum_mk,
-                                          rp_pm, cnt_pm, rp_mt, cnt_mt, list);
-    fill2_kernel<<<(EPM + EMT + 255) / 256, 256, 0, stream>>>(
-        src_pm, dst_pm, src_mt, dst_mt, rp_pm, cur_pm, csr_pm, rp_mt, cur_mt, csr_mt);
-
-    gatherpm_kernel<<<(NMHC + 7) / 8, 256, 0, stream>>>(rp_pm, csr_pm, emb_pep, Acat1, Acat2, NMHC);
-
-    mfma_fused_kernel<256, 2, true, true><<<dim3((NMHC + 127) / 128, 4), 256, 0, stream>>>(
-        NMHC, Acat1, Wcat1_b, l1_pm_bl, Acat2 + 128, 384, Zb1);
-    mfma_fused_kernel<384, 2, true, true><<<dim3((NMHC + 127) / 128, 4), 256, 0, stream>>>(
-        NMHC, Acat2, Wcat2_b, l2_pm_bl, mhc2_b, 256, Zb2);
-
-    tcrall_kernel<<<(MAXU + 31) / 32, 256, 0, stream>>>(
-        bsum_mk + 98, list, rp_mt, csr_mt, Zb1, Zb2, emb_tcr,
-        Wr1_b, Wr2_b, W1c_b, l1_mt_bl, l2_mt_bl, Ht_b);
-
-    mfma_out_kernel<128, true, true><<<dim3((NPEP + 127) / 128, 2), 256, 0, stream>>>(
-        NPEP, emb_pep, Wcomp_b, bp, Hp_b);
-    mfma_out_kernel<256, false, false><<<dim3((NMHC + 127) / 128, 2), 256, 0, stream>>>(
-        NMHC, mhc2_b, W1b_b, nullptr, Hm_b);
-
-    combine_kernel<<<(BB + 31) / 32, 256, 0, stream>>>(
-        Hp_b, Hm_b, Ht_b, pack_pep, pack_mhc, pack_tcr,
-        head_b1, head_W2, head_b2, out);
-}
+    a.deg_pm = ib;
+    a.cur_pm = ib + 5000;
+    a.deg_mt = ib + 10000;
+    a.cur_mt = ib + 110000;
+    a.mark   = ib + 210000;
+    a.rp_pm  = ib + 310000;
+    a.rp_mt  = ib + 315008;
+    a.csr_pm = ib + 415016;
+    a.csr_mt = ib + 615016;
+    a.bsum_pm = ib + 1015016;
+    a.bsum_mt = ib + 1015176;
+    a.bsum_mk = ib + 1015336;
+    a.nrows   = ib + 1015496;
+    a.list    = ib + 1015504;
+    a.bar     = ib + 1065552;
+
+    float* f = (float*)(ib + 1065568);
+    a.bp = f;
+
+    ushort* u = (ushort*)(f + 256);
+    a.Wcat1_b = u;
+    a.Wcat2_b = u + 131072;
+    a.W1b_b   = u + 327680;
+    a.W1c_b   = u + 393216;
+    a.Wcomp_b = u + 458752;
+    a.Wr1_b   = u + 491520;
+    a.Wr2_b   = u + 524288;
+    a.Acat1   = u + 589824;
+    a.Acat2   = u + 1869824;
+    a.Zb1     = u + 3789824;
+    a.Zb2     = u + 5069824;
+    a.mhc2_b  = u + 6349824;
+    a.Hp_b    = u + 7629824;
+    a.Hm_b    = u + 12749824;
+    a.Ht_b    = u + 14029824;
+
+    static int nblk = 0;
+    if (nblk == 0) {
+        int occ = 0, ncu = 0;
+        hipDeviceProp_t prop;
+        if (hipGetDeviceProperties(&prop, 0) == hipSuccess) ncu = prop.multiProcessorCount;
+        if (ncu <= 0) ncu = 256;
+        if (hipOccupancyMaxActiveBlocksPerMultiprocessor(&occ, mega_kernel, 256, 0) != hipSuccess || occ <= 0)
+            occ = 1;
+        if (occ > 3) occ = 3;
+        nblk = occ * ncu;
+        if (nblk > 768) nblk = 768;
+        if (nblk < 8) nblk = 8;
+    }
+
+    hipMemsetAsync(a.bar, 0, 16, stream);
+    mega_kernel<<<nblk, 256, 0, stream>>>(a);
+}
```

After: 1.138 ms. +173.4%, slower.
